# Optimization experiments

Measured on AMD Instinct MI355X. Metric: run time of the kernel, lower is better.

Reference implementation:

```python
import jax, jax.numpy as jnp
import numpy as np
import math

N, S, E, H = 32, 64, 512, 4
HD = E // H
EQ = E // 4
L2_TEMP = 13.544
LN_EPS = 1e-5


def _ln(x, g, b):
    m = jnp.mean(x, -1, keepdims=True)
    v = jnp.var(x, -1, keepdims=True)
    return (x - m) * jax.lax.rsqrt(v + LN_EPS) * g + b


def setup_inputs() -> dict:
    key = jax.random.key(0)
    ks = jax.random.split(key, 16)
    sc = 0.02
    inp = {
        "x": jax.random.normal(ks[0], (N, S, E), jnp.float32),
        # MultiheadAttention params (torch layout: in_proj_weight (3E,E))
        "Wqkv": jax.random.normal(ks[1], (3 * E, E), jnp.float32) * sc,
        "bqkv": jnp.zeros((3 * E,), jnp.float32),
        "Wo": jax.random.normal(ks[2], (E, E), jnp.float32) * sc,
        "bo": jnp.zeros((E,), jnp.float32),
        # fc1 (E, 2E), fc2 (E, E)
        "W1": jax.random.normal(ks[3], (E, 2 * E), jnp.float32) * sc,
        "b1": jnp.zeros((E,), jnp.float32),
        "W2": jax.random.normal(ks[4], (E, E), jnp.float32) * sc,
        "b2": jnp.zeros((E,), jnp.float32),
        # layer norms
        "g1": jnp.ones((E,), jnp.float32), "be1": jnp.zeros((E,), jnp.float32),
        "g2": jnp.ones((E,), jnp.float32), "be2": jnp.zeros((E,), jnp.float32),
        # fc_diff1: Linear(E, E//4), Linear(E//4, 1)
        "d1W1": jax.random.normal(ks[5], (EQ, E), jnp.float32) * sc,
        "d1b1": jnp.zeros((EQ,), jnp.float32),
        "d1W2": jax.random.normal(ks[6], (1, EQ), jnp.float32) * sc,
        "d1b2": jnp.zeros((1,), jnp.float32),
        # fc_diff2
        "d2W1": jax.random.normal(ks[7], (EQ, E), jnp.float32) * sc,
        "d2b1": jnp.zeros((EQ,), jnp.float32),
        "d2W2": jax.random.normal(ks[8], (1, EQ), jnp.float32) * sc,
        "d2b2": jnp.zeros((1,), jnp.float32),
    }
    return inp


def _mha(x, Wqkv, bqkv, Wo, bo):
    n, s, e = x.shape
    qkv = x @ Wqkv.T + bqkv
    q, k, v = jnp.split(qkv, 3, axis=-1)
    sh = lambda t: t.reshape(n, s, H, HD).transpose(0, 2, 1, 3)  # (n,H,s,hd)
    q, k, v = sh(q), sh(k), sh(v)
    scores = jnp.einsum('bhqd,bhkd->bhqk', q, k) / math.sqrt(HD)
    a = jax.nn.softmax(scores, axis=-1)
    o = jnp.einsum('bhqk,bhkd->bhqd', a, v).transpose(0, 2, 1, 3).reshape(n, s, e)
    return o @ Wo.T + bo, a.mean(axis=1)  # averaged attn weights (torch default)


def _pair_mlp(diff_w, W1a, b1a, W2a, b2a):
    # F.relu applied after every 'layer' (Linear, Dropout(eval=id), Linear)
    h = jax.nn.relu(diff_w @ W1a.T + b1a)  # relu(dropout(relu)) == relu composed -> same
    return jax.nn.relu(h @ W2a.T + b2a)[..., 0]  # (N,f,f)


def reference(x, Wqkv, bqkv, Wo, bo, W1, b1, W2, b2, g1, be1, g2, be2,
              d1W1, d1b1, d1W2, d1b2, d2W1, d2b1, d2W2, d2b2):
    # diff[b,f,g,e] = x[b,g,e] - x[b,f,e]
    diff = x[:, None, :, :] - x[:, :, None, :]  # (N,f,f,E)
    x1_attn = jax.nn.softmax(-jnp.sum(diff * diff, -1) / L2_TEMP, axis=-1)  # (N,f,f)
    x1 = jnp.einsum('bfg,bge->bfe', x1_attn, x)
    x2, x2_attn = _mha(x, Wqkv, bqkv, Wo, bo)
    x_res = jnp.concatenate([x1, x2], axis=-1)
    h = x + jax.nn.relu(x_res @ W1.T + b1)  # dropout eval = identity
    h = _ln(h, g1, be1)
    h = h + jax.nn.relu(h @ W2.T + b2)
    out = _ln(h, g2, be2)
    diff1 = _pair_mlp(diff * x1_attn[..., None], d1W1, d1b1, d1W2, d1b2)
    diff2 = _pair_mlp(diff * x2_attn[..., None], d2W1, d2b1, d2W2, d2b2)
    return out, x1_attn[:, None], x2_attn[:, None], diff1, diff2
```

## Files before the change

kernel.cpp:

```cpp
#include <hip/hip_runtime.h>
#include <math.h>

#define SS 64
#define EE 512
#define L2T 13.544f
#define LNEPS 1e-5f

using bf16x8 = __attribute__((ext_vector_type(8))) __bf16;
using u16x8  = __attribute__((ext_vector_type(8))) unsigned short;
using f32x4  = __attribute__((ext_vector_type(4))) float;

typedef const void __attribute__((address_space(1))) cv_global;
typedef void __attribute__((address_space(3))) v_lds;

__device__ inline unsigned short f2bf(float f) {
    union { float f; unsigned u; } v; v.f = f;
    unsigned r = v.u + 0x7fff + ((v.u >> 16) & 1);
    return (unsigned short)(r >> 16);
}
__device__ inline float bf2f(unsigned short h) {
    union { unsigned u; float f; } v; v.u = (unsigned)h << 16;
    return v.f;
}

#define MFMA16 __builtin_amdgcn_mfma_f32_16x16x32_bf16

#define XB_O    0
#define WFULL_O 1048576
#define W1CB_O  1966080
#define W2B_O   2490368
#define QKVB_O  2752512
#define X1O_O   5898240
#define HB_O    7995392
#define PB_O    9043968

__global__ __launch_bounds__(256)
void mega1(const float* __restrict__ x, const float* __restrict__ Wqkv,
           const float* __restrict__ Wo, const float* __restrict__ W1,
           const float* __restrict__ W2, const float* __restrict__ d1,
           const float* __restrict__ d2, const float* __restrict__ b1,
           const float* __restrict__ bo, unsigned short* __restrict__ bb,
           float* __restrict__ b_eff, float* __restrict__ x1_attn,
           unsigned short* __restrict__ Pl2) {
    const int bx = blockIdx.x, tid = threadIdx.x;
    __shared__ __align__(16) char smem[36096];

    if (bx < 1408) {
        int i = bx * 256 + tid;
        ushort4* dst4 = (ushort4*)bb;
        const float4* s; int di;
        if (i < 196608)      { s = (const float4*)Wqkv + i;          di = WFULL_O/4 + i; }
        else if (i < 212992) { int j = i-196608; s = (const float4*)d1 + j; di = WFULL_O/4 + 196608 + j; }
        else if (i < 229376) { int j = i-212992; s = (const float4*)d2 + j; di = WFULL_O/4 + 212992 + j; }
        else if (i < 294912) { int j = i-229376; s = (const float4*)W2 + j; di = W2B_O/4 + j; }
        else                 { int j = i-294912; int r = j>>7, cq = j&127;
                               s = (const float4*)W1 + r*256 + cq;   di = W1CB_O/4 + r*256 + cq; }
        float4 v = *s;
        ushort4 o;
        o.x = f2bf(v.x); o.y = f2bf(v.y); o.z = f2bf(v.z); o.w = f2bf(v.w);
        dst4[di] = o;
    } else if (bx < 1472) {
        const int tb = bx - 1408;
        const int m0 = (tb >> 3) * 64, n0 = (tb & 7) * 64;
        unsigned short* Asl = (unsigned short*)smem;
        unsigned short* Bsl = Asl + 64 * 40;
        const int wave = tid >> 6, lane = tid & 63;
        const int wm = (wave >> 1) * 32, wn = (wave & 1) * 32;
        const int fr = lane & 15, kq = (lane >> 4) * 8;
        f32x4 acc[2][2] = {};
        for (int k0 = 0; k0 < 512; k0 += 32) {
            {
                int m = tid >> 2, kk = (tid & 3) * 8;
                const float* src = W1 + (size_t)(m0 + m) * 1024 + 512 + k0 + kk;
                float4 v0 = *(const float4*)src, v1 = *(const float4*)(src + 4);
                u16x8 t = {f2bf(v0.x), f2bf(v0.y), f2bf(v0.z), f2bf(v0.w),
                           f2bf(v1.x), f2bf(v1.y), f2bf(v1.z), f2bf(v1.w)};
                *(u16x8*)(Asl + m * 40 + kk) = t;
            }
            {
                int k = tid >> 3, jq = (tid & 7) * 8;
                const float* src = Wo + (size_t)(k0 + k) * 512 + n0 + jq;
                float4 v0 = *(const float4*)src, v1 = *(const float4*)(src + 4);
                float vv[8] = {v0.x, v0.y, v0.z, v0.w, v1.x, v1.y, v1.z, v1.w};
                #pragma unroll
                for (int e = 0; e < 8; ++e) Bsl[(jq + e) * 40 + k] = f2bf(vv[e]);
            }
            __syncthreads();
            bf16x8 a0 = *(const bf16x8*)(Asl + (wm + fr) * 40 + kq);
            bf16x8 a1 = *(const bf16x8*)(Asl + (wm + 16 + fr) * 40 + kq);
            bf16x8 b0 = *(const bf16x8*)(Bsl + (wn + fr) * 40 + kq);
            bf16x8 b1 = *(const bf16x8*)(Bsl + (wn + 16 + fr) * 40 + kq);
            acc[0][0] = MFMA16(a0, b0, acc[0][0], 0, 0, 0);
            acc[0][1] = MFMA16(a0, b1, acc[0][1], 0, 0, 0);
            acc[1][0] = MFMA16(a1, b0, acc[1][0], 0, 0, 0);
            acc[1][1] = MFMA16(a1, b1, acc[1][1], 0, 0, 0);
            __syncthreads();
        }
        unsigned short* W1cb = bb + W1CB_O;
        const int crow = (lane >> 4) * 4, ccol = lane & 15;
        #pragma unroll
        for (int r2 = 0; r2 < 2; ++r2)
            #pragma unroll
            for (int c2 = 0; c2 < 2; ++c2)
                #pragma unroll
                for (int i = 0; i < 4; ++i) {
                    int m = m0 + wm + r2 * 16 + crow + i;
                    int j = n0 + wn + c2 * 16 + ccol;
                    W1cb[(size_t)m * 1024 + 512 + j] = f2bf(acc[r2][c2][i]);
                }
    } else if (bx < 1476) {
        int n = (bx - 1472) * 128 + (tid >> 1);
        int kh = (tid & 1) * 256;
        float s = 0.f;
        for (int k = 0; k < 256; ++k)
            s += W1[(size_t)n * 1024 + 512 + kh + k] * bo[kh + k];
        s += __shfl_xor(s, 1);
        if ((tid & 1) == 0) b_eff[n] = b1[n] + s;
    } else {
        const int b = bx - 1476;
        unsigned short* Xhi = (unsigned short*)smem;
        unsigned short* Xlo = Xhi + 64 * 72;
        float* sc    = (float*)(Xlo + 64 * 72);
        float* norms = sc + 64 * 68;
        const int wave = tid >> 6, lane = tid & 63;
        const int wm = (wave >> 1) * 32, wn = (wave & 1) * 32;
        const int fr = lane & 15;
        const int srow = tid >> 2, scq = (tid & 3) * 16;

        f32x4 acc[2][2] = {};
        const float* xrow = x + (size_t)b * 32768;
        unsigned short* xbg = bb + XB_O + (size_t)b * 32768;

        for (int k0 = 0; k0 < 512; k0 += 64) {
            const float* src = xrow + srow * 512 + k0 + scq;
            u16x8 hi0, hi1, lo0, lo1;
            #pragma unroll
            for (int e = 0; e < 8; ++e) {
                float v = src[e];
                unsigned short h = f2bf(v);
                hi0[e] = h; lo0[e] = f2bf(v - bf2f(h));
            }
            #pragma unroll
            for (int e = 0; e < 8; ++e) {
                float v = src[8 + e];
                unsigned short h = f2bf(v);
                hi1[e] = h; lo1[e] = f2bf(v - bf2f(h));
            }
            *(u16x8*)(Xhi + srow * 72 + scq)     = hi0;
            *(u16x8*)(Xhi + srow * 72 + scq + 8) = hi1;
            *(u16x8*)(Xlo + srow * 72 + scq)     = lo0;
            *(u16x8*)(Xlo + srow * 72 + scq + 8) = lo1;
            *(u16x8*)(xbg + srow * 512 + k0 + scq)     = hi0;
            *(u16x8*)(xbg + srow * 512 + k0 + scq + 8) = hi1;
            __syncthreads();
            #pragma unroll
            for (int j = 0; j < 2; ++j) {
                int kk = j * 32 + (lane >> 4) * 8;
                bf16x8 ah0 = *(const bf16x8*)(Xhi + (wm + fr) * 72 + kk);
                bf16x8 ah1 = *(const bf16x8*)(Xhi + (wm + 16 + fr) * 72 + kk);
                bf16x8 bh0 = *(const bf16x8*)(Xhi + (wn + fr) * 72 + kk);
                bf16x8 bh1 = *(const bf16x8*)(Xhi + (wn + 16 + fr) * 72 + kk);
                bf16x8 al0 = *(const bf16x8*)(Xlo + (wm + fr) * 72 + kk);
                bf16x8 al1 = *(const bf16x8*)(Xlo + (wm + 16 + fr) * 72 + kk);
                bf16x8 bl0 = *(const bf16x8*)(Xlo + (wn + fr) * 72 + kk);
                bf16x8 bl1 = *(const bf16x8*)(Xlo + (wn + 16 + fr) * 72 + kk);
                acc[0][0] = MFMA16(ah0, bh0, acc[0][0], 0, 0, 0);
                acc[0][0] = MFMA16(ah0, bl0, acc[0][0], 0, 0, 0);
                acc[0][0] = MFMA16(al0, bh0, acc[0][0], 0, 0, 0);
                acc[0][1] = MFMA16(ah0, bh1, acc[0][1], 0, 0, 0);
                acc[0][1] = MFMA16(ah0, bl1, acc[0][1], 0, 0, 0);
                acc[0][1] = MFMA16(al0, bh1, acc[0][1], 0, 0, 0);
                acc[1][0] = MFMA16(ah1, bh0, acc[1][0], 0, 0, 0);
                acc[1][0] = MFMA16(ah1, bl0, acc[1][0], 0, 0, 0);
                acc[1][0] = MFMA16(al1, bh0, acc[1][0], 0, 0, 0);
                acc[1][1] = MFMA16(ah1, bh1, acc[1][1], 0, 0, 0);
                acc[1][1] = MFMA16(ah1, bl1, acc[1][1], 0, 0, 0);
                acc[1][1] = MFMA16(al1, bh1, acc[1][1], 0, 0, 0);
            }
            __syncthreads();
        }
        const int crow = (lane >> 4) * 4, ccol = lane & 15;
        #pragma unroll
        for (int r2 = 0; r2 < 2; ++r2)
            #pragma unroll
            for (int c2 = 0; c2 < 2; ++c2)
                #pragma unroll
                for (int i = 0; i < 4; ++i)
                    sc[(wm + r2 * 16 + crow + i) * 68 + wn + c2 * 16 + ccol] =
                        acc[r2][c2][i];
        __syncthreads();
        if (tid < 64) norms[tid] = sc[tid * 68 + tid];
        __syncthreads();
        #pragma unroll
        for (int i = 0; i < 16; ++i) {
            int f = wave * 16 + i;
            float nf = norms[f];
            float val = (2.f * sc[f * 68 + lane] - nf - norms[lane]) * (1.0f / L2T);
            float mx = val;
            #pragma unroll
            for (int m = 32; m; m >>= 1) mx = fmaxf(mx, __shfl_xor(mx, m));
            float e = expf(val - mx);
            float sum = e;
            #pragma unroll
            for (int m = 32; m; m >>= 1) sum += __shfl_xor(sum, m);
            float a = e / sum;
            x1_attn[((size_t)b * 64 + f) * 64 + lane] = a;
            Pl2[((size_t)b * 64 + f) * 64 + lane] = f2bf(a);
        }
    }
}

__global__ __launch_bounds__(256)
void gemm_qkvp(const unsigned short* __restrict__ A,
               const unsigned short* __restrict__ B,
               const float* __restrict__ bias,
               unsigned short* __restrict__ Cq, unsigned short* __restrict__ Cp,
               const unsigned short* __restrict__ Pl2,
               unsigned short* __restrict__ x1o) {
    __shared__ unsigned short qsm[8704];
    const int tid = threadIdx.x, wave = tid >> 6, lane = tid & 63;
    const int fr = lane & 15;
    const int crow = (lane >> 4) * 4, ccol = lane & 15;

    if (blockIdx.x < 28) {
        unsigned short* Asl = qsm;
        unsigned short* Bsl = qsm + 4096;
        const int m0 = blockIdx.y * 64, n0 = blockIdx.x * 64;
        const int wm = (wave >> 1) * 32, wn = (wave & 1) * 32;
        const int kq4 = lane >> 4;
        f32x4 acc[2][2] = {};

        for (int k0 = 0; k0 < 512; k0 += 64) {
            #pragma unroll
            for (int c0 = 0; c0 < 512; c0 += 256) {
                int cc = c0 + tid, r = cc >> 3, q = cc & 7;
                int col = (q ^ (r & 7)) * 8;
                __builtin_amdgcn_global_load_lds(
                    (cv_global*)(A + (size_t)(m0 + r) * 512 + k0 + col),
                    (v_lds*)(Asl + c0 * 8 + wave * 512), 16, 0, 0);
            }
            #pragma unroll
            for (int c0 = 0; c0 < 512; c0 += 256) {
                int cc = c0 + tid, r = cc >> 3, q = cc & 7;
                int col = (q ^ (r & 7)) * 8;
                __builtin_amdgcn_global_load_lds(
                    (cv_global*)(B + (size_t)(n0 + r) * 512 + k0 + col),
                    (v_lds*)(Bsl + c0 * 8 + wave * 512), 16, 0, 0);
            }
            __syncthreads();
            #pragma unroll
            for (int j = 0; j < 2; ++j) {
                int kc = kq4 + j * 4;
                int rb0 = wn + fr, rb1 = wn + 16 + fr;
                bf16x8 b0 = *(const bf16x8*)(Bsl + rb0 * 64 + (kc ^ (rb0 & 7)) * 8);
                bf16x8 b1 = *(const bf16x8*)(Bsl + rb1 * 64 + (kc ^ (rb1 & 7)) * 8);
                #pragma unroll
                for (int r = 0; r < 2; ++r) {
                    int ra = wm + r * 16 + fr;
                    bf16x8 af = *(const bf16x8*)(Asl + ra * 64 + (kc ^ (ra & 7)) * 8);
                    acc[r][0] = MFMA16(af, b0, acc[r][0], 0, 0, 0);
                    acc[r][1] = MFMA16(af, b1, acc[r][1], 0, 0, 0);
                }
            }
            __syncthreads();
        }

        if (blockIdx.x < 24) {
            float bj0 = bias[n0 + wn + ccol], bj1 = bias[n0 + wn + 16 + ccol];
            #pragma unroll
            for (int r = 0; r < 2; ++r)
                #pragma unroll
                for (int c = 0; c < 2; ++c) {
                    float bj = c ? bj1 : bj0;
                    #pragma unroll
                    for (int i = 0; i < 4; ++i) {
                        size_t m = (size_t)(m0 + wm + r * 16 + crow + i);
                        int n = n0 + wn + c * 16 + ccol;
                        Cq[m * 1536 + n] = f2bf(acc[r][c][i] + bj);
                    }
                }
        } else {
            int p0 = n0 - 1536;
            #pragma unroll
            for (int r = 0; r < 2; ++r)
                #pragma unroll
                for (int c = 0; c < 2; ++c)
                    #pragma unroll
                    for (int i = 0; i < 4; ++i) {
                        size_t m = (size_t)(m0 + wm + r * 16 + crow + i);
                        int n = p0 + wn + c * 16 + ccol;
                        Cp[m * 256 + n] = f2bf(acc[r][c][i]);
                    }
        }
    } else {
        const int e0 = (blockIdx.x - 28) * 64;
        const int b = blockIdx.y;
        unsigned short* Ap = qsm;
        unsigned short* Xt = qsm + 64 * 68;
        {
            int row = tid >> 2, cq = (tid & 3) * 16;
            const unsigned short* src = Pl2 + (size_t)b * 4096 + row * 64 + cq;
            *(u16x8*)(Ap + row * 68 + cq)     = *(const u16x8*)src;
            *(u16x8*)(Ap + row * 68 + cq + 8) = *(const u16x8*)(src + 8);
        }
        {
            int g = tid >> 2, cq = (tid & 3) * 16;
            const unsigned short* src = A + (size_t)b * 32768 + g * 512 + e0 + cq;
            u16x8 v0 = *(const u16x8*)src, v1 = *(const u16x8*)(src + 8);
            #pragma unroll
            for (int e = 0; e < 8; ++e) Xt[(cq + e) * 68 + g] = v0[e];
            #pragma unroll
            for (int e = 0; e < 8; ++e) Xt[(cq + 8 + e) * 68 + g] = v1[e];
        }
        __syncthreads();
        const int wm2 = wave * 16;
        f32x4 o[4] = {};
        #pragma unroll
        for (int j = 0; j < 2; ++j) {
            int kk = j * 32 + (lane >> 4) * 8;
            bf16x8 a = *(const bf16x8*)(Ap + (wm2 + fr) * 68 + kk);
            #pragma unroll
            for (int t = 0; t < 4; ++t) {
                bf16x8 bv = *(const bf16x8*)(Xt + (t * 16 + fr) * 68 + kk);
                o[t] = MFMA16(a, bv, o[t], 0, 0, 0);
            }
        }
        #pragma unroll
        for (int t = 0; t < 4; ++t)
            #pragma unroll
            for (int i = 0; i < 4; ++i) {
                size_t m = (size_t)b * 64 + wm2 + crow + i;
                x1o[m * 1024 + e0 + t * 16 + ccol] = f2bf(o[t][i]);
            }
    }
}

__global__ __launch_bounds__(256)
void mha_attn(const unsigned short* __restrict__ qkv,
              unsigned short* __restrict__ x1o, float* __restrict__ pws) {
    const int hh = blockIdx.x;
    const int h = hh >> 1, half = hh & 1;
    const int b = blockIdx.y;
    const int tid = threadIdx.x, wave = tid >> 6, lane = tid & 63;

    __shared__ unsigned short Qs[32 * 136];
    __shared__ unsigned short Ks[64 * 136];
    __shared__ unsigned short Vt[128 * 72];
    __shared__ float sc[32 * 68];
    __shared__ unsigned short Pbf[32 * 72];

    const unsigned short* base = qkv + (size_t)b * 64 * 1536;
    {
        int row = tid >> 3, col = (tid & 7) * 16;
        const unsigned short* src = base + (half * 32 + row) * 1536 + h * 128 + col;
        *(u16x8*)(Qs + row * 136 + col)     = *(const u16x8*)(src);
        *(u16x8*)(Qs + row * 136 + col + 8) = *(const u16x8*)(src + 8);
    }
    {
        int row = tid >> 2, col = (tid & 3) * 32;
        const unsigned short* src = base + row * 1536 + 512 + h * 128 + col;
        #pragma unroll
        for (int j = 0; j < 4; ++j)
            *(u16x8*)(Ks + row * 136 + col + j * 8) = *(const u16x8*)(src + j * 8);
    }
    {
        int g = tid >> 2, col = (tid & 3) * 32;
        const unsigned short* src = base + g * 1536 + 1024 + h * 128 + col;
        #pragma unroll
        for (int j = 0; j < 4; ++j) {
            u16x8 v = *(const u16x8*)(src + j * 8);
            #pragma unroll
            for (int e = 0; e < 8; ++e)
                Vt[(col + j * 8 + e) * 72 + g] = v[e];
        }
    }
    __syncthreads();

    const int fr = lane & 15, kq = (lane >> 4) * 8;
    const int crow = (lane >> 4) * 4, ccol = lane & 15;
    const int wm = (wave >> 1) * 16;
    {
        const int wn = (wave & 1) * 32;
        f32x4 s0 = {0.f, 0.f, 0.f, 0.f}, s1 = s0;
        #pragma unroll
        for (int k0 = 0; k0 < 128; k0 += 32) {
            bf16x8 a  = *(const bf16x8*)(Qs + (wm + fr) * 136 + k0 + kq);
            bf16x8 b0 = *(const bf16x8*)(Ks + (wn + fr) * 136 + k0 + kq);
            bf16x8 b1 = *(const bf16x8*)(Ks + (wn + 16 + fr) * 136 + k0 + kq);
            s0 = MFMA16(a, b0, s0, 0, 0, 0);
            s1 = MFMA16(a, b1, s1, 0, 0, 0);
        }
        const float scale = 0.08838834764831845f;
        #pragma unroll
        for (int r = 0; r < 4; ++r) {
            sc[(wm + crow + r) * 68 + wn + ccol]      = s0[r] * scale;
            sc[(wm + crow + r) * 68 + wn + 16 + ccol] = s1[r] * scale;
        }
    }
    __syncthreads();

    #pragma unroll
    for (int i = 0; i < 8; ++i) {
        int f = wave * 8 + i;
        float v = sc[f * 68 + lane];
        float mx = v;
        #pragma unroll
        for (int m = 32; m; m >>= 1) mx = fmaxf(mx, __shfl_xor(mx, m));
        float e = expf(v - mx);
        float sum = e;
        #pragma unroll
        for (int m = 32; m; m >>= 1) sum += __shfl_xor(sum, m);
        float a = e / sum;
        Pbf[f * 72 + lane] = f2bf(a);
        pws[(((size_t)b * 4 + h) * 64 + half * 32 + f) * 64 + lane] = a;
    }
    __syncthreads();

    {
        const int wn2 = (wave & 1) * 64;
        f32x4 o[4];
        #pragma unroll
        for (int t = 0; t < 4; ++t) o[t] = f32x4{0.f, 0.f, 0.f, 0.f};
        #pragma unroll
        for (int k0 = 0; k0 < 64; k0 += 32) {
            bf16x8 a = *(const bf16x8*)(Pbf + (wm + fr) * 72 + k0 + kq);
            #pragma unroll
            for (int t = 0; t < 4; ++t) {
                bf16x8 bv = *(const bf16x8*)(Vt + (wn2 + t * 16 + fr) * 72 + k0 + kq);
                o[t] = MFMA16(a, bv, o[t], 0, 0, 0);
            }
        }
        #pragma unroll
        for (int t = 0; t < 4; ++t)
            #pragma unroll
            for (int r = 0; r < 4; ++r) {
                size_t m = (size_t)b * 64 + half * 32 + wm + crow + r;
                int col = h * 128 + wn2 + t * 16 + ccol;
                x1o[m * 1024 + 512 + col] = f2bf(o[t][r]);
            }
    }
}

__global__ __launch_bounds__(256)
void w1pair(const unsigned short* __restrict__ x1o,
            const unsigned short* __restrict__ W1cb,
            const float* __restrict__ beff, float* __restrict__ u,
            const unsigned short* __restrict__ Pb,
            const float* __restrict__ a1, const float* __restrict__ pws,
            const float* __restrict__ d1b1, const float* __restrict__ d1w2,
            const float* __restrict__ d1b2, const float* __restrict__ d2b1,
            const float* __restrict__ d2w2, const float* __restrict__ d2b2,
            float* __restrict__ x2_attn, float* __restrict__ out1,
            float* __restrict__ out2) {
    __shared__ unsigned short Asl[32 * 64];
    __shared__ unsigned short Bsl[64 * 64];
    const int bx = blockIdx.x, tid = threadIdx.x;
    const int wave = tid >> 6, lane = tid & 63;

    if (bx < 512) {
        const int m0 = (bx >> 3) * 32, n0 = (bx & 7) * 64;
        const int wm = (wave >> 1) * 16, wn = (wave & 1) * 32;
        const int fr = lane & 15, kq4 = lane >> 4;
        f32x4 acc[2] = {};
        for (int k0 = 0; k0 < 1024; k0 += 64) {
            {
                int r = tid >> 3, q = tid & 7;
                int col = (q ^ (r & 7)) * 8;
                __builtin_amdgcn_global_load_lds(
                    (cv_global*)(x1o + (size_t)(m0 + r) * 1024 + k0 + col),
                    (v_lds*)(Asl + wave * 512), 16, 0, 0);
            }
            #pragma unroll
            for (int c0 = 0; c0 < 512; c0 += 256) {
                int cc = c0 + tid, r = cc >> 3, q = cc & 7;
                int col = (q ^ (r & 7)) * 8;
                __builtin_amdgcn_global_load_lds(
                    (cv_global*)(W1cb + (size_t)(n0 + r) * 1024 + k0 + col),
                    (v_lds*)(Bsl + c0 * 8 + wave * 512), 16, 0, 0);
            }
            __syncthreads();
            #pragma unroll
            for (int j = 0; j < 2; ++j) {
                int kc = kq4 + j * 4;
                int rb0 = wn + fr, rb1 = wn + 16 + fr, ra = wm + fr;
                bf16x8 b0 = *(const bf16x8*)(Bsl + rb0 * 64 + (kc ^ (rb0 & 7)) * 8);
                bf16x8 b1 = *(const bf16x8*)(Bsl + rb1 * 64 + (kc ^ (rb1 & 7)) * 8);
                bf16x8 af = *(const bf16x8*)(Asl + ra * 64 + (kc ^ (ra & 7)) * 8);
                acc[0] = MFMA16(af, b0, acc[0], 0, 0, 0);
                acc[1] = MFMA16(af, b1, acc[1], 0, 0, 0);
            }
            __syncthreads();
        }
        const int crow = (lane >> 4) * 4, ccol = lane & 15;
        #pragma unroll
        for (int c = 0; c < 2; ++c) {
            int n = n0 + wn + c * 16 + ccol;
            float bj = beff[n];
            #pragma unroll
            for (int i = 0; i < 4; ++i) {
                size_t m = (size_t)(m0 + wm + crow + i);
                u[m * 512 + n] = fmaxf(acc[c][i] + bj, 0.f);
            }
        }
    } else {
        const int idx = bx - 512;
        const int f = idx & 63, b = idx >> 6;
        const size_t row = (size_t)b * SS + f;
        const int c0 = lane * 2, c1 = lane * 2 + 1;

        const float p1f0 = bf2f(Pb[row * 256 + c0]),       p1f1 = bf2f(Pb[row * 256 + c1]);
        const float p2f0 = bf2f(Pb[row * 256 + 128 + c0]), p2f1 = bf2f(Pb[row * 256 + 128 + c1]);
        const float w10 = d1w2[c0], w11 = d1w2[c1];
        const float w20 = d2w2[c0], w21 = d2w2[c1];
        const float b10 = d1b1[c0], b11 = d1b1[c1];
        const float b20 = d2b1[c0], b21 = d2b1[c1];
        const float bb1 = d1b2[0], bb2 = d2b2[0];

        const float* a1r = a1 + row * SS;
        const float* ph0 = pws + (((size_t)b * 4 + 0) * 64 + f) * 64;
        const float* ph1 = pws + (((size_t)b * 4 + 1) * 64 + f) * 64;
        const float* ph2 = pws + (((size_t)b * 4 + 2) * 64 + f) * 64;
        const float* ph3 = pws + (((size_t)b * 4 + 3) * 64 + f) * 64;
        const size_t bbase = (size_t)b * SS * 256;

        for (int g = wave; g < 64; g += 4) {
            float aa1 = a1r[g];
            float aa2 = 0.25f * (ph0[g] + ph1[g] + ph2[g] + ph3[g]);
            float q10 = bf2f(Pb[bbase + g * 256 + c0]);
            float q11 = bf2f(Pb[bbase + g * 256 + c1]);
            float q20 = bf2f(Pb[bbase + g * 256 + 128 + c0]);
            float q21 = bf2f(Pb[bbase + g * 256 + 128 + c1]);
            float h10 = fmaxf(aa1 * (q10 - p1f0) + b10, 0.f);
            float h11 = fmaxf(aa1 * (q11 - p1f1) + b11, 0.f);
            float h20 = fmaxf(aa2 * (q20 - p2f0) + b20, 0.f);
            float h21 = fmaxf(aa2 * (q21 - p2f1) + b21, 0.f);
            float s1 = w10 * h10 + w11 * h11;
            float s2 = w20 * h20 + w21 * h21;
            #pragma unroll
            for (int m = 32; m; m >>= 1) {
                s1 += __shfl_xor(s1, m);
                s2 += __shfl_xor(s2, m);
            }
            if (lane == 0) {
                x2_attn[row * SS + g] = aa2;
                out1[row * SS + g] = fmaxf(s1 + bb1, 0.f);
                out2[row * SS + g] = fmaxf(s2 + bb2, 0.f);
            }
        }
    }
}

__global__ __launch_bounds__(256)
void gemm_w2(const unsigned short* __restrict__ A,
             const unsigned short* __restrict__ B,
             const float* __restrict__ bias, float* __restrict__ C) {
    __shared__ unsigned short Asl[32 * 64];
    __shared__ unsigned short Bsl[64 * 64];
    const int tid = threadIdx.x, wave = tid >> 6, lane = tid & 63;
    const int m0 = blockIdx.y * 32, n0 = blockIdx.x * 64;
    const int wm = (wave >> 1) * 16, wn = (wave & 1) * 32;
    const int fr = lane & 15, kq4 = lane >> 4;
    f32x4 acc[2] = {};
    for (int k0 = 0; k0 < 512; k0 += 64) {
        {
            int r = tid >> 3, q = tid & 7;
            int col = (q ^ (r & 7)) * 8;
            __builtin_amdgcn_global_load_lds(
                (cv_global*)(A + (size_t)(m0 + r) * 512 + k0 + col),
                (v_lds*)(Asl + wave * 512), 16, 0, 0);
        }
        #pragma unroll
        for (int c0 = 0; c0 < 512; c0 += 256) {
            int cc = c0 + tid, r = cc >> 3, q = cc & 7;
            int col = (q ^ (r & 7)) * 8;
            __builtin_amdgcn_global_load_lds(
                (cv_global*)(B + (size_t)(n0 + r) * 512 + k0 + col),
                (v_lds*)(Bsl + c0 * 8 + wave * 512), 16, 0, 0);
        }
        __syncthreads();
        #pragma unroll
        for (int j = 0; j < 2; ++j) {
            int kc = kq4 + j * 4;
            int rb0 = wn + fr, rb1 = wn + 16 + fr, ra = wm + fr;
            bf16x8 b0 = *(const bf16x8*)(Bsl + rb0 * 64 + (kc ^ (rb0 & 7)) * 8);
            bf16x8 b1 = *(const bf16x8*)(Bsl + rb1 * 64 + (kc ^ (rb1 & 7)) * 8);
            bf16x8 af = *(const bf16x8*)(Asl + ra * 64 + (kc ^ (ra & 7)) * 8);
            acc[0] = MFMA16(af, b0, acc[0], 0, 0, 0);
            acc[1] = MFMA16(af, b1, acc[1], 0, 0, 0);
        }
        __syncthreads();
    }
    const int crow = (lane >> 4) * 4, ccol = lane & 15;
    #pragma unroll
    for (int c = 0; c < 2; ++c) {
        int n = n0 + wn + c * 16 + ccol;
        float bj = bias[n];
        #pragma unroll
        for (int i = 0; i < 4; ++i) {
            size_t m = (size_t)(m0 + wm + crow + i);
            C[m * 512 + n] = fmaxf(acc[c][i] + bj, 0.f);
        }
    }
}

__global__ __launch_bounds__(256)
void add_ln(const float* __restrict__ base, const float* __restrict__ u,
            const float* __restrict__ gam, const float* __restrict__ bet,
            float* __restrict__ out, unsigned short* __restrict__ outb) {
    const int row = blockIdx.x;
    const int tid = threadIdx.x, wave = tid >> 6, lane = tid & 63;
    const float* br = base + (size_t)row * EE;
    const float* ur = u + (size_t)row * EE;
    float t0 = br[tid] + ur[tid];
    float t1 = br[tid + 256] + ur[tid + 256];
    float s = t0 + t1, sq = t0 * t0 + t1 * t1;
    #pragma unroll
    for (int m = 32; m; m >>= 1) {
        s += __shfl_xor(s, m);
        sq += __shfl_xor(sq, m);
    }
    __shared__ float ssum[4], ssq[4];
    if (lane == 0) { ssum[wave] = s; ssq[wave] = sq; }
    __syncthreads();
    s = ssum[0] + ssum[1] + ssum[2] + ssum[3];
    sq = ssq[0] + ssq[1] + ssq[2] + ssq[3];
    float mean = s * (1.0f / EE);
    float var = sq * (1.0f / EE) - mean * mean;
    float inv = rsqrtf(var + LNEPS);
    float v0 = (t0 - mean) * inv * gam[tid] + bet[tid];
    float v1 = (t1 - mean) * inv * gam[tid + 256] + bet[tid + 256];
    float* orow = out + (size_t)row * EE;
    orow[tid] = v0;
    orow[tid + 256] = v1;
    if (outb) {
        unsigned short* obr = outb + (size_t)row * EE;
        obr[tid] = f2bf(v0);
        obr[tid + 256] = f2bf(v1);
    }
}

extern "C" void kernel_launch(void* const* d_in, const int* in_sizes, int n_in,
                              void* d_out, int out_size, void* d_ws,
                              size_t ws_size, hipStream_t stream) {
    const float* x    = (const float*)d_in[0];
    const float* Wqkv = (const float*)d_in[1];
    const float* bqkv = (const float*)d_in[2];
    const float* Wo   = (const float*)d_in[3];
    const float* bo   = (const float*)d_in[4];
    const float* W1   = (const float*)d_in[5];
    const float* b1   = (const float*)d_in[6];
    const float* W2   = (const float*)d_in[7];
    const float* b2   = (const float*)d_in[8];
    const float* g1   = (const float*)d_in[9];
    const float* be1  = (const float*)d_in[10];
    const float* g2   = (const float*)d_in[11];
    const float* be2  = (const float*)d_in[12];
    const float* d1W1 = (const float*)d_in[13];
    const float* d1b1 = (const float*)d_in[14];
    const float* d1W2 = (const float*)d_in[15];
    const float* d1b2 = (const float*)d_in[16];
    const float* d2W1 = (const float*)d_in[17];
    const float* d2b1 = (const float*)d_in[18];
    const float* d2W2 = (const float*)d_in[19];
    const float* d2b2 = (const float*)d_in[20];

    float* out      = (float*)d_out;
    float* out_main = out;
    float* x1_attn  = out + 1048576;
    float* x2_attn  = out + 1048576 + 131072;
    float* diff1    = out + 1048576 + 2 * 131072;
    float* diff2    = out + 1048576 + 3 * 131072;

    float* ws    = (float*)d_ws;
    float* u_buf = ws;
    float* h_buf = ws + 1048576;
    float* pws   = ws + 2097152;
    float* b_eff = ws + 2621440;
    unsigned short* Pl2 = (unsigned short*)(ws + 2621952);
    unsigned short* bb  = (unsigned short*)(ws + 2687488);

    unsigned short* xb    = bb + XB_O;
    unsigned short* Wfull = bb + WFULL_O;
    unsigned short* W1cb  = bb + W1CB_O;
    unsigned short* W2b   = bb + W2B_O;
    unsigned short* qkvb  = bb + QKVB_O;
    unsigned short* x1o   = bb + X1O_O;
    unsigned short* hb    = bb + HB_O;
    unsigned short* Pb    = bb + PB_O;

    mega1<<<1508, 256, 0, stream>>>(x, Wqkv, Wo, W1, W2, d1W1, d2W1, b1, bo,
                                    bb, b_eff, x1_attn, Pl2);

    gemm_qkvp<<<dim3(36, 32), 256, 0, stream>>>(xb, Wfull, bqkv, qkvb, Pb,
                                                Pl2, x1o);

    mha_attn<<<dim3(8, 32), 256, 0, stream>>>(qkvb, x1o, pws);

    w1pair<<<2560, 256, 0, stream>>>(x1o, W1cb, b_eff, u_buf, Pb, x1_attn, pws,
                                     d1b1, d1W2, d1b2, d2b1, d2W2, d2b2,
                                     x2_attn, diff1, diff2);

    add_ln<<<2048, 256, 0, stream>>>(x, u_buf, g1, be1, h_buf, hb);

    gemm_w2<<<dim3(8, 64), 256, 0, stream>>>(hb, W2b, b2, u_buf);

    add_ln<<<2048, 256, 0, stream>>>(h_buf, u_buf, g2, be2, out_main, nullptr);
}
```

Baseline: 179.0 us.

## Merge all seven kernel launches into one persistent cooperative kernel with grid syncs

```diff
diff --git a/kernel.cpp b/kernel.cpp
--- a/kernel.cpp
+++ b/kernel.cpp
@@ -1,5 +1,8 @@
 #include <hip/hip_runtime.h>
+#include <hip/hip_cooperative_groups.h>
 #include <math.h>
+
+namespace cg = cooperative_groups;
 
 #define SS 64
 #define EE 512
@@ -34,580 +37,18 @@
 #define HB_O    7995392
 #define PB_O    9043968
 
-__global__ __launch_bounds__(256)
-void mega1(const float* __restrict__ x, const float* __restrict__ Wqkv,
-           const float* __restrict__ Wo, const float* __restrict__ W1,
-           const float* __restrict__ W2, const float* __restrict__ d1,
-           const float* __restrict__ d2, const float* __restrict__ b1,
-           const float* __restrict__ bo, unsigned short* __restrict__ bb,
-           float* __restrict__ b_eff, float* __restrict__ x1_attn,
-           unsigned short* __restrict__ Pl2) {
-    const int bx = blockIdx.x, tid = threadIdx.x;
-    __shared__ __align__(16) char smem[36096];
-
-    if (bx < 1408) {
-        int i = bx * 256 + tid;
-        ushort4* dst4 = (ushort4*)bb;
-        const float4* s; int di;
-        if (i < 196608)      { s = (const float4*)Wqkv + i;          di = WFULL_O/4 + i; }
-        else if (i < 212992) { int j = i-196608; s = (const float4*)d1 + j; di = WFULL_O/4 + 196608 + j; }
-        else if (i < 229376) { int j = i-212992; s = (const float4*)d2 + j; di = WFULL_O/4 + 212992 + j; }
-        else if (i < 294912) { int j = i-229376; s = (const float4*)W2 + j; di = W2B_O/4 + j; }
-        else                 { int j = i-294912; int r = j>>7, cq = j&127;
-                               s = (const float4*)W1 + r*256 + cq;   di = W1CB_O/4 + r*256 + cq; }
-        float4 v = *s;
-        ushort4 o;
-        o.x = f2bf(v.x); o.y = f2bf(v.y); o.z = f2bf(v.z); o.w = f2bf(v.w);
-        dst4[di] = o;
-    } else if (bx < 1472) {
-        const int tb = bx - 1408;
-        const int m0 = (tb >> 3) * 64, n0 = (tb & 7) * 64;
-        unsigned short* Asl = (unsigned short*)smem;
-        unsigned short* Bsl = Asl + 64 * 40;
-        const int wave = tid >> 6, lane = tid & 63;
-        const int wm = (wave >> 1) * 32, wn = (wave & 1) * 32;
-        const int fr = lane & 15, kq = (lane >> 4) * 8;
-        f32x4 acc[2][2] = {};
-        for (int k0 = 0; k0 < 512; k0 += 32) {
-            {
-                int m = tid >> 2, kk = (tid & 3) * 8;
-                const float* src = W1 + (size_t)(m0 + m) * 1024 + 512 + k0 + kk;
-                float4 v0 = *(const float4*)src, v1 = *(const float4*)(src + 4);
-                u16x8 t = {f2bf(v0.x), f2bf(v0.y), f2bf(v0.z), f2bf(v0.w),
-                           f2bf(v1.x), f2bf(v1.y), f2bf(v1.z), f2bf(v1.w)};
-                *(u16x8*)(Asl + m * 40 + kk) = t;
-            }
-            {
-                int k = tid >> 3, jq = (tid & 7) * 8;
-                const float* src = Wo + (size_t)(k0 + k) * 512 + n0 + jq;
-                float4 v0 = *(const float4*)src, v1 = *(const float4*)(src + 4);
-                float vv[8] = {v0.x, v0.y, v0.z, v0.w, v1.x, v1.y, v1.z, v1.w};
-                #pragma unroll
-                for (int e = 0; e < 8; ++e) Bsl[(jq + e) * 40 + k] = f2bf(vv[e]);
-            }
-            __syncthreads();
-            bf16x8 a0 = *(const bf16x8*)(Asl + (wm + fr) * 40 + kq);
-            bf16x8 a1 = *(const bf16x8*)(Asl + (wm + 16 + fr) * 40 + kq);
-            bf16x8 b0 = *(const bf16x8*)(Bsl + (wn + fr) * 40 + kq);
-            bf16x8 b1 = *(const bf16x8*)(Bsl + (wn + 16 + fr) * 40 + kq);
-            acc[0][0] = MFMA16(a0, b0, acc[0][0], 0, 0, 0);
-            acc[0][1] = MFMA16(a0, b1, acc[0][1], 0, 0, 0);
-            acc[1][0] = MFMA16(a1, b0, acc[1][0], 0, 0, 0);
-            acc[1][1] = MFMA16(a1, b1, acc[1][1], 0, 0, 0);
-            __syncthreads();
-        }
-        unsigned short* W1cb = bb + W1CB_O;
-        const int crow = (lane >> 4) * 4, ccol = lane & 15;
-        #pragma unroll
-        for (int r2 = 0; r2 < 2; ++r2)
-            #pragma unroll
-            for (int c2 = 0; c2 < 2; ++c2)
-                #pragma unroll
-                for (int i = 0; i < 4; ++i) {
-                    int m = m0 + wm + r2 * 16 + crow + i;
-                    int j = n0 + wn + c2 * 16 + ccol;
-                    W1cb[(size_t)m * 1024 + 512 + j] = f2bf(acc[r2][c2][i]);
-                }
-    } else if (bx < 1476) {
-        int n = (bx - 1472) * 128 + (tid >> 1);
-        int kh = (tid & 1) * 256;
-        float s = 0.f;
-        for (int k = 0; k < 256; ++k)
-            s += W1[(size_t)n * 1024 + 512 + kh + k] * bo[kh + k];
-        s += __shfl_xor(s, 1);
-        if ((tid & 1) == 0) b_eff[n] = b1[n] + s;
-    } else {
-        const int b = bx - 1476;
-        unsigned short* Xhi = (unsigned short*)smem;
-        unsigned short* Xlo = Xhi + 64 * 72;
-        float* sc    = (float*)(Xlo + 64 * 72);
-        float* norms = sc + 64 * 68;
-        const int wave = tid >> 6, lane = tid & 63;
-        const int wm = (wave >> 1) * 32, wn = (wave & 1) * 32;
-        const int fr = lane & 15;
-        const int srow = tid >> 2, scq = (tid & 3) * 16;
-
-        f32x4 acc[2][2] = {};
-        const float* xrow = x + (size_t)b * 32768;
-        unsigned short* xbg = bb + XB_O + (size_t)b * 32768;
-
-        for (int k0 = 0; k0 < 512; k0 += 64) {
-            const float* src = xrow + srow * 512 + k0 + scq;
-            u16x8 hi0, hi1, lo0, lo1;
-            #pragma unroll
-            for (int e = 0; e < 8; ++e) {
-                float v = src[e];
-                unsigned short h = f2bf(v);
-                hi0[e] = h; lo0[e] = f2bf(v - bf2f(h));
-            }
-            #pragma unroll
-            for (int e = 0; e < 8; ++e) {
-                float v = src[8 + e];
-                unsigned short h = f2bf(v);
-                hi1[e] = h; lo1[e] = f2bf(v - bf2f(h));
-            }
-            *(u16x8*)(Xhi + srow * 72 + scq)     = hi0;
-            *(u16x8*)(Xhi + srow * 72 + scq + 8) = hi1;
-            *(u16x8*)(Xlo + srow * 72 + scq)     = lo0;
-            *(u16x8*)(Xlo + srow * 72 + scq + 8) = lo1;
-            *(u16x8*)(xbg + srow * 512 + k0 + scq)     = hi0;
-            *(u16x8*)(xbg + srow * 512 + k0 + scq + 8) = hi1;
-            __syncthreads();
-            #pragma unroll
-            for (int j = 0; j < 2; ++j) {
-                int kk = j * 32 + (lane >> 4) * 8;
-                bf16x8 ah0 = *(const bf16x8*)(Xhi + (wm + fr) * 72 + kk);
-                bf16x8 ah1 = *(const bf16x8*)(Xhi + (wm + 16 + fr) * 72 + kk);
-                bf16x8 bh0 = *(const bf16x8*)(Xhi + (wn + fr) * 72 + kk);
-                bf16x8 bh1 = *(const bf16x8*)(Xhi + (wn + 16 + fr) * 72 + kk);
-                bf16x8 al0 = *(const bf16x8*)(Xlo + (wm + fr) * 72 + kk);
-                bf16x8 al1 = *(const bf16x8*)(Xlo + (wm + 16 + fr) * 72 + kk);
-                bf16x8 bl0 = *(const bf16x8*)(Xlo + (wn + fr) * 72 + kk);
-                bf16x8 bl1 = *(const bf16x8*)(Xlo + (wn + 16 + fr) * 72 + kk);
-                acc[0][0] = MFMA16(ah0, bh0, acc[0][0], 0, 0, 0);
-                acc[0][0] = MFMA16(ah0, bl0, acc[0][0], 0, 0, 0);
-                acc[0][0] = MFMA16(al0, bh0, acc[0][0], 0, 0, 0);
-                acc[0][1] = MFMA16(ah0, bh1, acc[0][1], 0, 0, 0);
-                acc[0][1] = MFMA16(ah0, bl1, acc[0][1], 0, 0, 0);
-                acc[0][1] = MFMA16(al0, bh1, acc[0][1], 0, 0, 0);
-                acc[1][0] = MFMA16(ah1, bh0, acc[1][0], 0, 0, 0);
-                acc[1][0] = MFMA16(ah1, bl0, acc[1][0], 0, 0, 0);
-                acc[1][0] = MFMA16(al1, bh0, acc[1][0], 0, 0, 0);
-                acc[1][1] = MFMA16(ah1, bh1, acc[1][1], 0, 0, 0);
-                acc[1][1] = MFMA16(ah1, bl1, acc[1][1], 0, 0, 0);
-                acc[1][1] = MFMA16(al1, bh1, acc[1][1], 0, 0, 0);
-            }
-            __syncthreads();
-        }
-        const int crow = (lane >> 4) * 4, ccol = lane & 15;
-        #pragma unroll
-        for (int r2 = 0; r2 < 2; ++r2)
-            #pragma unroll
-            for (int c2 = 0; c2 < 2; ++c2)
-                #pragma unroll
-                for (int i = 0; i < 4; ++i)
-                    sc[(wm + r2 * 16 + crow + i) * 68 + wn + c2 * 16 + ccol] =
-                        acc[r2][c2][i];
-        __syncthreads();
-        if (tid < 64) norms[tid] = sc[tid * 68 + tid];
-        __syncthreads();
-        #pragma unroll
-        for (int i = 0; i < 16; ++i) {
-            int f = wave * 16 + i;
-            float nf = norms[f];
-            float val = (2.f * sc[f * 68 + lane] - nf - norms[lane]) * (1.0f / L2T);
-            float mx = val;
-            #pragma unroll
-            for (int m = 32; m; m >>= 1) mx = fmaxf(mx, __shfl_xor(mx, m));
-            float e = expf(val - mx);
-            float sum = e;
-            #pragma unroll
-            for (int m = 32; m; m >>= 1) sum += __shfl_xor(sum, m);
-            float a = e / sum;
-            x1_attn[((size_t)b * 64 + f) * 64 + lane] = a;
-            Pl2[((size_t)b * 64 + f) * 64 + lane] = f2bf(a);
-        }
-    }
-}
-
-__global__ __launch_bounds__(256)
-void gemm_qkvp(const unsigned short* __restrict__ A,
-               const unsigned short* __restrict__ B,
-               const float* __restrict__ bias,
-               unsigned short* __restrict__ Cq, unsigned short* __restrict__ Cp,
-               const unsigned short* __restrict__ Pl2,
-               unsigned short* __restrict__ x1o) {
-    __shared__ unsigned short qsm[8704];
-    const int tid = threadIdx.x, wave = tid >> 6, lane = tid & 63;
-    const int fr = lane & 15;
-    const int crow = (lane >> 4) * 4, ccol = lane & 15;
-
-    if (blockIdx.x < 28) {
-        unsigned short* Asl = qsm;
-        unsigned short* Bsl = qsm + 4096;
-        const int m0 = blockIdx.y * 64, n0 = blockIdx.x * 64;
-        const int wm = (wave >> 1) * 32, wn = (wave & 1) * 32;
-        const int kq4 = lane >> 4;
-        f32x4 acc[2][2] = {};
-
-        for (int k0 = 0; k0 < 512; k0 += 64) {
-            #pragma unroll
-            for (int c0 = 0; c0 < 512; c0 += 256) {
-                int cc = c0 + tid, r = cc >> 3, q = cc & 7;
-                int col = (q ^ (r & 7)) * 8;
-                __builtin_amdgcn_global_load_lds(
-                    (cv_global*)(A + (size_t)(m0 + r) * 512 + k0 + col),
-                    (v_lds*)(Asl + c0 * 8 + wave * 512), 16, 0, 0);
-            }
-            #pragma unroll
-            for (int c0 = 0; c0 < 512; c0 += 256) {
-                int cc = c0 + tid, r = cc >> 3, q = cc & 7;
-                int col = (q ^ (r & 7)) * 8;
-                __builtin_amdgcn_global_load_lds(
-                    (cv_global*)(B + (size_t)(n0 + r) * 512 + k0 + col),
-                    (v_lds*)(Bsl + c0 * 8 + wave * 512), 16, 0, 0);
-            }
-            __syncthreads();
-            #pragma unroll
-            for (int j = 0; j < 2; ++j) {
-                int kc = kq4 + j * 4;
-                int rb0 = wn + fr, rb1 = wn + 16 + fr;
-                bf16x8 b0 = *(const bf16x8*)(Bsl + rb0 * 64 + (kc ^ (rb0 & 7)) * 8);
-                bf16x8 b1 = *(const bf16x8*)(Bsl + rb1 * 64 + (kc ^ (rb1 & 7)) * 8);
-                #pragma unroll
-                for (int r = 0; r < 2; ++r) {
-                    int ra = wm + r * 16 + fr;
-                    bf16x8 af = *(const bf16x8*)(Asl + ra * 64 + (kc ^ (ra & 7)) * 8);
-                    acc[r][0] = MFMA16(af, b0, acc[r][0], 0, 0, 0);
-                    acc[r][1] = MFMA16(af, b1, acc[r][1], 0, 0, 0);
-                }
-            }
-            __syncthreads();
-        }
-
-        if (blockIdx.x < 24) {
-            float bj0 = bias[n0 + wn + ccol], bj1 = bias[n0 + wn + 16 + ccol];
-            #pragma unroll
-            for (int r = 0; r < 2; ++r)
-                #pragma unroll
-                for (int c = 0; c < 2; ++c) {
-                    float bj = c ? bj1 : bj0;
-                    #pragma unroll
-                    for (int i = 0; i < 4; ++i) {
-                        size_t m = (size_t)(m0 + wm + r * 16 + crow + i);
-                        int n = n0 + wn + c * 16 + ccol;
-                        Cq[m * 1536 + n] = f2bf(acc[r][c][i] + bj);
-                    }
-                }
-        } else {
-            int p0 = n0 - 1536;
-            #pragma unroll
-            for (int r = 0; r < 2; ++r)
-                #pragma unroll
-                for (int c = 0; c < 2; ++c)
-                    #pragma unroll
-                    for (int i = 0; i < 4; ++i) {
-                        size_t m = (size_t)(m0 + wm + r * 16 + crow + i);
-                        int n = p0 + wn + c * 16 + ccol;
-                        Cp[m * 256 + n] = f2bf(acc[r][c][i]);
-                    }
-        }
-    } else {
-        const int e0 = (blockIdx.x - 28) * 64;
-        const int b = blockIdx.y;
-        unsigned short* Ap = qsm;
-        unsigned short* Xt = qsm + 64 * 68;
-        {
-            int row = tid >> 2, cq = (tid & 3) * 16;
-            const unsigned short* src = Pl2 + (size_t)b * 4096 + row * 64 + cq;
-            *(u16x8*)(Ap + row * 68 + cq)     = *(const u16x8*)src;
-            *(u16x8*)(Ap + row * 68 + cq + 8) = *(const u16x8*)(src + 8);
-        }
-        {
-            int g = tid >> 2, cq = (tid & 3) * 16;
-            const unsigned short* src = A + (size_t)b * 32768 + g * 512 + e0 + cq;
-            u16x8 v0 = *(const u16x8*)src, v1 = *(const u16x8*)(src + 8);
-            #pragma unroll
-            for (int e = 0; e < 8; ++e) Xt[(cq + e) * 68 + g] = v0[e];
-            #pragma unroll
-            for (int e = 0; e < 8; ++e) Xt[(cq + 8 + e) * 68 + g] = v1[e];
-        }
-        __syncthreads();
-        const int wm2 = wave * 16;
-        f32x4 o[4] = {};
-        #pragma unroll
-        for (int j = 0; j < 2; ++j) {
-            int kk = j * 32 + (lane >> 4) * 8;
-            bf16x8 a = *(const bf16x8*)(Ap + (wm2 + fr) * 68 + kk);
-            #pragma unroll
-            for (int t = 0; t < 4; ++t) {
-                bf16x8 bv = *(const bf16x8*)(Xt + (t * 16 + fr) * 68 + kk);
-                o[t] = MFMA16(a, bv, o[t], 0, 0, 0);
-            }
-        }
-        #pragma unroll
-        for (int t = 0; t < 4; ++t)
-            #pragma unroll
-            for (int i = 0; i < 4; ++i) {
-                size_t m = (size_t)b * 64 + wm2 + crow + i;
-                x1o[m * 1024 + e0 + t * 16 + ccol] = f2bf(o[t][i]);
-            }
-    }
-}
-
-__global__ __launch_bounds__(256)
-void mha_attn(const unsigned short* __restrict__ qkv,
-              unsigned short* __restrict__ x1o, float* __restrict__ pws) {
-    const int hh = blockIdx.x;
-    const int h = hh >> 1, half = hh & 1;
-    const int b = blockIdx.y;
-    const int tid = threadIdx.x, wave = tid >> 6, lane = tid & 63;
-
-    __shared__ unsigned short Qs[32 * 136];
-    __shared__ unsigned short Ks[64 * 136];
-    __shared__ unsigned short Vt[128 * 72];
-    __shared__ float sc[32 * 68];
-    __shared__ unsigned short Pbf[32 * 72];
-
-    const unsigned short* base = qkv + (size_t)b * 64 * 1536;
-    {
-        int row = tid >> 3, col = (tid & 7) * 16;
-        const unsigned short* src = base + (half * 32 + row) * 1536 + h * 128 + col;
-        *(u16x8*)(Qs + row * 136 + col)     = *(const u16x8*)(src);
-        *(u16x8*)(Qs + row * 136 + col + 8) = *(const u16x8*)(src + 8);
-    }
-    {
-        int row = tid >> 2, col = (tid & 3) * 32;
-        const unsigned short* src = base + row * 1536 + 512 + h * 128 + col;
-        #pragma unroll
-        for (int j = 0; j < 4; ++j)
-            *(u16x8*)(Ks + row * 136 + col + j * 8) = *(const u16x8*)(src + j * 8);
-    }
-    {
-        int g = tid >> 2, col = (tid & 3) * 32;
-        const unsigned short* src = base + g * 1536 + 1024 + h * 128 + col;
-        #pragma unroll
-        for (int j = 0; j < 4; ++j) {
-            u16x8 v = *(const u16x8*)(src + j * 8);
-            #pragma unroll
-            for (int e = 0; e < 8; ++e)
-                Vt[(col + j * 8 + e) * 72 + g] = v[e];
-        }
-    }
-    __syncthreads();
-
-    const int fr = lane & 15, kq = (lane >> 4) * 8;
-    const int crow = (lane >> 4) * 4, ccol = lane & 15;
-    const int wm = (wave >> 1) * 16;
-    {
-        const int wn = (wave & 1) * 32;
-        f32x4 s0 = {0.f, 0.f, 0.f, 0.f}, s1 = s0;
-        #pragma unroll
-        for (int k0 = 0; k0 < 128; k0 += 32) {
-            bf16x8 a  = *(const bf16x8*)(Qs + (wm + fr) * 136 + k0 + kq);
-            bf16x8 b0 = *(const bf16x8*)(Ks + (wn + fr) * 136 + k0 + kq);
-            bf16x8 b1 = *(const bf16x8*)(Ks + (wn + 16 + fr) * 136 + k0 + kq);
-            s0 = MFMA16(a, b0, s0, 0, 0, 0);
-            s1 = MFMA16(a, b1, s1, 0, 0, 0);
-        }
-        const float scale = 0.08838834764831845f;
-        #pragma unroll
-        for (int r = 0; r < 4; ++r) {
-            sc[(wm + crow + r) * 68 + wn + ccol]      = s0[r] * scale;
-            sc[(wm + crow + r) * 68 + wn + 16 + ccol] = s1[r] * scale;
-        }
-    }
-    __syncthreads();
-
-    #pragma unroll
-    for (int i = 0; i < 8; ++i) {
-        int f = wave * 8 + i;
-        float v = sc[f * 68 + lane];
-        float mx = v;
-        #pragma unroll
-        for (int m = 32; m; m >>= 1) mx = fmaxf(mx, __shfl_xor(mx, m));
-        float e = expf(v - mx);
-        float sum = e;
-        #pragma unroll
-        for (int m = 32; m; m >>= 1) sum += __shfl_xor(sum, m);
-        float a = e / sum;
-        Pbf[f * 72 + lane] = f2bf(a);
-        pws[(((size_t)b * 4 + h) * 64 + half * 32 + f) * 64 + lane] = a;
-    }
-    __syncthreads();
-
-    {
-        const int wn2 = (wave & 1) * 64;
-        f32x4 o[4];
-        #pragma unroll
-        for (int t = 0; t < 4; ++t) o[t] = f32x4{0.f, 0.f, 0.f, 0.f};
-        #pragma unroll
-        for (int k0 = 0; k0 < 64; k0 += 32) {
-            bf16x8 a = *(const bf16x8*)(Pbf + (wm + fr) * 72 + k0 + kq);
-            #pragma unroll
-            for (int t = 0; t < 4; ++t) {
-                bf16x8 bv = *(const bf16x8*)(Vt + (wn2 + t * 16 + fr) * 72 + k0 + kq);
-                o[t] = MFMA16(a, bv, o[t], 0, 0, 0);
-            }
-        }
-        #pragma unroll
-        for (int t = 0; t < 4; ++t)
-            #pragma unroll
-            for (int r = 0; r < 4; ++r) {
-                size_t m = (size_t)b * 64 + half * 32 + wm + crow + r;
-                int col = h * 128 + wn2 + t * 16 + ccol;
-                x1o[m * 1024 + 512 + col] = f2bf(o[t][r]);
-            }
-    }
-}
-
-__global__ __launch_bounds__(256)
-void w1pair(const unsigned short* __restrict__ x1o,
-            const unsigned short* __restrict__ W1cb,
-            const float* __restrict__ beff, float* __restrict__ u,
-            const unsigned short* __restrict__ Pb,
-            const float* __restrict__ a1, const float* __restrict__ pws,
-            const float* __restrict__ d1b1, const float* __restrict__ d1w2,
-            const float* __restrict__ d1b2, const float* __restrict__ d2b1,
-            const float* __restrict__ d2w2, const float* __restrict__ d2b2,
-            float* __restrict__ x2_attn, float* __restrict__ out1,
-            float* __restrict__ out2) {
-    __shared__ unsigned short Asl[32 * 64];
-    __shared__ unsigned short Bsl[64 * 64];
-    const int bx = blockIdx.x, tid = threadIdx.x;
-    const int wave = tid >> 6, lane = tid & 63;
-
-    if (bx < 512) {
-        const int m0 = (bx >> 3) * 32, n0 = (bx & 7) * 64;
-        const int wm = (wave >> 1) * 16, wn = (wave & 1) * 32;
-        const int fr = lane & 15, kq4 = lane >> 4;
-        f32x4 acc[2] = {};
-        for (int k0 = 0; k0 < 1024; k0 += 64) {
-            {
-                int r = tid >> 3, q = tid & 7;
-                int col = (q ^ (r & 7)) * 8;
-                __builtin_amdgcn_global_load_lds(
-                    (cv_global*)(x1o + (size_t)(m0 + r) * 1024 + k0 + col),
-                    (v_lds*)(Asl + wave * 512), 16, 0, 0);
-            }
-            #pragma unroll
-            for (int c0 = 0; c0 < 512; c0 += 256) {
-                int cc = c0 + tid, r = cc >> 3, q = cc & 7;
-                int col = (q ^ (r & 7)) * 8;
-                __builtin_amdgcn_global_load_lds(
-                    (cv_global*)(W1cb + (size_t)(n0 + r) * 1024 + k0 + col),
-                    (v_lds*)(Bsl + c0 * 8 + wave * 512), 16, 0, 0);
-            }
-            __syncthreads();
-            #pragma unroll
-            for (int j = 0; j < 2; ++j) {
-                int kc = kq4 + j * 4;
-                int rb0 = wn + fr, rb1 = wn + 16 + fr, ra = wm + fr;
-                bf16x8 b0 = *(const bf16x8*)(Bsl + rb0 * 64 + (kc ^ (rb0 & 7)) * 8);
-                bf16x8 b1 = *(const bf16x8*)(Bsl + rb1 * 64 + (kc ^ (rb1 & 7)) * 8);
-                bf16x8 af = *(const bf16x8*)(Asl + ra * 64 + (kc ^ (ra & 7)) * 8);
-                acc[0] = MFMA16(af, b0, acc[0], 0, 0, 0);
-                acc[1] = MFMA16(af, b1, acc[1], 0, 0, 0);
-            }
-            __syncthreads();
-        }
-        const int crow = (lane >> 4) * 4, ccol = lane & 15;
-        #pragma unroll
-        for (int c = 0; c < 2; ++c) {
-            int n = n0 + wn + c * 16 + ccol;
-            float bj = beff[n];
-            #pragma unroll
-            for (int i = 0; i < 4; ++i) {
-                size_t m = (size_t)(m0 + wm + crow + i);
-                u[m * 512 + n] = fmaxf(acc[c][i] + bj, 0.f);
-            }
-        }
-    } else {
-        const int idx = bx - 512;
-        const int f = idx & 63, b = idx >> 6;
-        const size_t row = (size_t)b * SS + f;
-        const int c0 = lane * 2, c1 = lane * 2 + 1;
-
-        const float p1f0 = bf2f(Pb[row * 256 + c0]),       p1f1 = bf2f(Pb[row * 256 + c1]);
-        const float p2f0 = bf2f(Pb[row * 256 + 128 + c0]), p2f1 = bf2f(Pb[row * 256 + 128 + c1]);
-        const float w10 = d1w2[c0], w11 = d1w2[c1];
-        const float w20 = d2w2[c0], w21 = d2w2[c1];
-        const float b10 = d1b1[c0], b11 = d1b1[c1];
-        const float b20 = d2b1[c0], b21 = d2b1[c1];
-        const float bb1 = d1b2[0], bb2 = d2b2[0];
-
-        const float* a1r = a1 + row * SS;
-        const float* ph0 = pws + (((size_t)b * 4 + 0) * 64 + f) * 64;
-        const float* ph1 = pws + (((size_t)b * 4 + 1) * 64 + f) * 64;
-        const float* ph2 = pws + (((size_t)b * 4 + 2) * 64 + f) * 64;
-        const float* ph3 = pws + (((size_t)b * 4 + 3) * 64 + f) * 64;
-        const size_t bbase = (size_t)b * SS * 256;
-
-        for (int g = wave; g < 64; g += 4) {
-            float aa1 = a1r[g];
-            float aa2 = 0.25f * (ph0[g] + ph1[g] + ph2[g] + ph3[g]);
-            float q10 = bf2f(Pb[bbase + g * 256 + c0]);
-            float q11 = bf2f(Pb[bbase + g * 256 + c1]);
-            float q20 = bf2f(Pb[bbase + g * 256 + 128 + c0]);
-            float q21 = bf2f(Pb[bbase + g * 256 + 128 + c1]);
-            float h10 = fmaxf(aa1 * (q10 - p1f0) + b10, 0.f);
-            float h11 = fmaxf(aa1 * (q11 - p1f1) + b11, 0.f);
-            float h20 = fmaxf(aa2 * (q20 - p2f0) + b20, 0.f);
-            float h21 = fmaxf(aa2 * (q21 - p2f1) + b21, 0.f);
-            float s1 = w10 * h10 + w11 * h11;
-            float s2 = w20 * h20 + w21 * h21;
-            #pragma unroll
-            for (int m = 32; m; m >>= 1) {
-                s1 += __shfl_xor(s1, m);
-                s2 += __shfl_xor(s2, m);
-            }
-            if (lane == 0) {
-                x2_attn[row * SS + g] = aa2;
-                out1[row * SS + g] = fmaxf(s1 + bb1, 0.f);
-                out2[row * SS + g] = fmaxf(s2 + bb2, 0.f);
-            }
-        }
-    }
-}
-
-__global__ __launch_bounds__(256)
-void gemm_w2(const unsigned short* __restrict__ A,
-             const unsigned short* __restrict__ B,
-             const float* __restrict__ bias, float* __restrict__ C) {
-    __shared__ unsigned short Asl[32 * 64];
-    __shared__ unsigned short Bsl[64 * 64];
-    const int tid = threadIdx.x, wave = tid >> 6, lane = tid & 63;
-    const int m0 = blockIdx.y * 32, n0 = blockIdx.x * 64;
-    const int wm = (wave >> 1) * 16, wn = (wave & 1) * 32;
-    const int fr = lane & 15, kq4 = lane >> 4;
-    f32x4 acc[2] = {};
-    for (int k0 = 0; k0 < 512; k0 += 64) {
-        {
-            int r = tid >> 3, q = tid & 7;
-            int col = (q ^ (r & 7)) * 8;
-            __builtin_amdgcn_global_load_lds(
-                (cv_global*)(A + (size_t)(m0 + r) * 512 + k0 + col),
-                (v_lds*)(Asl + wave * 512), 16, 0, 0);
-        }
-        #pragma unroll
-        for (int c0 = 0; c0 < 512; c0 += 256) {
-            int cc = c0 + tid, r = cc >> 3, q = cc & 7;
-            int col = (q ^ (r & 7)) * 8;
-            __builtin_amdgcn_global_load_lds(
-                (cv_global*)(B + (size_t)(n0 + r) * 512 + k0 + col),
-                (v_lds*)(Bsl + c0 * 8 + wave * 512), 16, 0, 0);
-        }
-        __syncthreads();
-        #pragma unroll
-        for (int j = 0; j < 2; ++j) {
-            int kc = kq4 + j * 4;
-            int rb0 = wn + fr, rb1 = wn + 16 + fr, ra = wm + fr;
-            bf16x8 b0 = *(const bf16x8*)(Bsl + rb0 * 64 + (kc ^ (rb0 & 7)) * 8);
-            bf16x8 b1 = *(const bf16x8*)(Bsl + rb1 * 64 + (kc ^ (rb1 & 7)) * 8);
-            bf16x8 af = *(const bf16x8*)(Asl + ra * 64 + (kc ^ (ra & 7)) * 8);
-            acc[0] = MFMA16(af, b0, acc[0], 0, 0, 0);
-            acc[1] = MFMA16(af, b1, acc[1], 0, 0, 0);
-        }
-        __syncthreads();
-    }
-    const int crow = (lane >> 4) * 4, ccol = lane & 15;
-    #pragma unroll
-    for (int c = 0; c < 2; ++c) {
-        int n = n0 + wn + c * 16 + ccol;
-        float bj = bias[n];
-        #pragma unroll
-        for (int i = 0; i < 4; ++i) {
-            size_t m = (size_t)(m0 + wm + crow + i);
-            C[m * 512 + n] = fmaxf(acc[c][i] + bj, 0.f);
-        }
-    }
-}
-
-__global__ __launch_bounds__(256)
-void add_ln(const float* __restrict__ base, const float* __restrict__ u,
-            const float* __restrict__ gam, const float* __restrict__ bet,
-            float* __restrict__ out, unsigned short* __restrict__ outb) {
-    const int row = blockIdx.x;
+struct KParams {
+    const float *x, *Wqkv, *bqkv, *Wo, *bo, *W1, *b1, *W2, *b2;
+    const float *g1, *be1, *g2, *be2;
+    const float *d1W1, *d1b1, *d1W2, *d1b2, *d2W1, *d2b1, *d2W2, *d2b2;
+    float *out_main, *x1_attn, *x2_attn, *diff1, *diff2;
+    float *u_buf, *h_buf, *pws, *b_eff;
+    unsigned short *Pl2, *bb;
+};
+
+__device__ inline void ln_row(int row, const float* base, const float* u,
+                              const float* gam, const float* bet, float* out,
+                              unsigned short* outb, float* ssum, float* ssq) {
     const int tid = threadIdx.x, wave = tid >> 6, lane = tid & 63;
     const float* br = base + (size_t)row * EE;
     const float* ur = u + (size_t)row * EE;
@@ -619,7 +60,6 @@
         s += __shfl_xor(s, m);
         sq += __shfl_xor(sq, m);
     }
-    __shared__ float ssum[4], ssq[4];
     if (lane == 0) { ssum[wave] = s; ssq[wave] = sq; }
     __syncthreads();
     s = ssum[0] + ssum[1] + ssum[2] + ssum[3];
@@ -637,72 +77,602 @@
         obr[tid] = f2bf(v0);
         obr[tid + 256] = f2bf(v1);
     }
+    __syncthreads();
+}
+
+__global__ __launch_bounds__(256, 4)
+void fused(KParams p) {
+    __shared__ __align__(16) unsigned char smem[27680];
+    const int tid = threadIdx.x, wave = tid >> 6, lane = tid & 63;
+    const int fr = lane & 15, quad = lane >> 4, kq = quad * 8;
+    const int crow = quad * 4, ccol = fr;
+    const int GS = gridDim.x;
+    cg::grid_group grid = cg::this_grid();
+    unsigned short* bb = p.bb;
+
+    for (int w = blockIdx.x; w < 1508; w += GS) {
+        if (w < 1408) {
+            int i = w * 256 + tid;
+            ushort4* dst4 = (ushort4*)bb;
+            const float4* s; int di;
+            if (i < 196608)      { s = (const float4*)p.Wqkv + i;              di = WFULL_O/4 + i; }
+            else if (i < 212992) { int j = i-196608; s = (const float4*)p.d1W1 + j; di = WFULL_O/4 + 196608 + j; }
+            else if (i < 229376) { int j = i-212992; s = (const float4*)p.d2W1 + j; di = WFULL_O/4 + 212992 + j; }
+            else if (i < 294912) { int j = i-229376; s = (const float4*)p.W2 + j;   di = W2B_O/4 + j; }
+            else                 { int j = i-294912; int r = j>>7, cq = j&127;
+                                   s = (const float4*)p.W1 + r*256 + cq;       di = W1CB_O/4 + r*256 + cq; }
+            float4 v = *s;
+            ushort4 o;
+            o.x = f2bf(v.x); o.y = f2bf(v.y); o.z = f2bf(v.z); o.w = f2bf(v.w);
+            dst4[di] = o;
+        } else if (w < 1472) {
+            const int tb = w - 1408;
+            const int m0 = (tb >> 3) * 64, n0 = (tb & 7) * 64;
+            unsigned short* Asl = (unsigned short*)smem;
+            unsigned short* Bsl = Asl + 64 * 40;
+            const int wm = (wave >> 1) * 32, wn = (wave & 1) * 32;
+            f32x4 acc[2][2] = {};
+            for (int k0 = 0; k0 < 512; k0 += 32) {
+                {
+                    int m = tid >> 2, kk = (tid & 3) * 8;
+                    const float* src = p.W1 + (size_t)(m0 + m) * 1024 + 512 + k0 + kk;
+                    float4 v0 = *(const float4*)src, v1 = *(const float4*)(src + 4);
+                    u16x8 t = {f2bf(v0.x), f2bf(v0.y), f2bf(v0.z), f2bf(v0.w),
+                               f2bf(v1.x), f2bf(v1.y), f2bf(v1.z), f2bf(v1.w)};
+                    *(u16x8*)(Asl + m * 40 + kk) = t;
+                }
+                {
+                    int k = tid >> 3, jq = (tid & 7) * 8;
+                    const float* src = p.Wo + (size_t)(k0 + k) * 512 + n0 + jq;
+                    float4 v0 = *(const float4*)src, v1 = *(const float4*)(src + 4);
+                    float vv[8] = {v0.x, v0.y, v0.z, v0.w, v1.x, v1.y, v1.z, v1.w};
+                    #pragma unroll
+                    for (int e = 0; e < 8; ++e) Bsl[(jq + e) * 40 + k] = f2bf(vv[e]);
+                }
+                __syncthreads();
+                bf16x8 a0 = *(const bf16x8*)(Asl + (wm + fr) * 40 + kq);
+                bf16x8 a1 = *(const bf16x8*)(Asl + (wm + 16 + fr) * 40 + kq);
+                bf16x8 b0 = *(const bf16x8*)(Bsl + (wn + fr) * 40 + kq);
+                bf16x8 b1 = *(const bf16x8*)(Bsl + (wn + 16 + fr) * 40 + kq);
+                acc[0][0] = MFMA16(a0, b0, acc[0][0], 0, 0, 0);
+                acc[0][1] = MFMA16(a0, b1, acc[0][1], 0, 0, 0);
+                acc[1][0] = MFMA16(a1, b0, acc[1][0], 0, 0, 0);
+                acc[1][1] = MFMA16(a1, b1, acc[1][1], 0, 0, 0);
+                __syncthreads();
+            }
+            unsigned short* W1cb = bb + W1CB_O;
+            #pragma unroll
+            for (int r2 = 0; r2 < 2; ++r2)
+                #pragma unroll
+                for (int c2 = 0; c2 < 2; ++c2)
+                    #pragma unroll
+                    for (int i = 0; i < 4; ++i) {
+                        int m = m0 + wm + r2 * 16 + crow + i;
+                        int j = n0 + wn + c2 * 16 + ccol;
+                        W1cb[(size_t)m * 1024 + 512 + j] = f2bf(acc[r2][c2][i]);
+                    }
+        } else if (w < 1476) {
+            int n = (w - 1472) * 128 + (tid >> 1);
+            int kh = (tid & 1) * 256;
+            float s = 0.f;
+            for (int k = 0; k < 256; ++k)
+                s += p.W1[(size_t)n * 1024 + 512 + kh + k] * p.bo[kh + k];
+            s += __shfl_xor(s, 1);
+            if ((tid & 1) == 0) p.b_eff[n] = p.b1[n] + s;
+        } else {
+            const int b = w - 1476;
+            unsigned short* Xhi = (unsigned short*)smem;
+            unsigned short* Xlo = Xhi + 64 * 72;
+            float* norms = (float*)(smem + 18432);
+            const int wmg = wave * 16;
+            const int srow = tid >> 2, scq = (tid & 3) * 16;
+            f32x4 acc[4] = {};
+            const float* xrow = p.x + (size_t)b * 32768;
+            unsigned short* xbg = bb + XB_O + (size_t)b * 32768;
+
+            for (int k0 = 0; k0 < 512; k0 += 64) {
+                const float* src = xrow + srow * 512 + k0 + scq;
+                u16x8 hi0, hi1, lo0, lo1;
+                #pragma unroll
+                for (int e = 0; e < 8; ++e) {
+                    float v = src[e];
+                    unsigned short h = f2bf(v);
+                    hi0[e] = h; lo0[e] = f2bf(v - bf2f(h));
+                }
+                #pragma unroll
+                for (int e = 0; e < 8; ++e) {
+                    float v = src[8 + e];
+                    unsigned short h = f2bf(v);
+                    hi1[e] = h; lo1[e] = f2bf(v - bf2f(h));
+                }
+                *(u16x8*)(Xhi + srow * 72 + scq)     = hi0;
+                *(u16x8*)(Xhi + srow * 72 + scq + 8) = hi1;
+                *(u16x8*)(Xlo + srow * 72 + scq)     = lo0;
+                *(u16x8*)(Xlo + srow * 72 + scq + 8) = lo1;
+                *(u16x8*)(xbg + srow * 512 + k0 + scq)     = hi0;
+                *(u16x8*)(xbg + srow * 512 + k0 + scq + 8) = hi1;
+                __syncthreads();
+                #pragma unroll
+                for (int j = 0; j < 2; ++j) {
+                    int kk = j * 32 + kq;
+                    bf16x8 ah = *(const bf16x8*)(Xhi + (wmg + fr) * 72 + kk);
+                    bf16x8 al = *(const bf16x8*)(Xlo + (wmg + fr) * 72 + kk);
+                    #pragma unroll
+                    for (int t = 0; t < 4; ++t) {
+                        bf16x8 bh = *(const bf16x8*)(Xhi + (t * 16 + fr) * 72 + kk);
+                        bf16x8 bl = *(const bf16x8*)(Xlo + (t * 16 + fr) * 72 + kk);
+                        acc[t] = MFMA16(ah, bh, acc[t], 0, 0, 0);
+                        acc[t] = MFMA16(ah, bl, acc[t], 0, 0, 0);
+                        acc[t] = MFMA16(al, bh, acc[t], 0, 0, 0);
+                    }
+                }
+                __syncthreads();
+            }
+            #pragma unroll
+            for (int t = 0; t < 4; ++t)
+                #pragma unroll
+                for (int r = 0; r < 4; ++r) {
+                    int row = wmg + crow + r, col = t * 16 + fr;
+                    if (row == col) norms[row] = acc[t][r];
+                }
+            __syncthreads();
+            float ncol[4];
+            #pragma unroll
+            for (int t = 0; t < 4; ++t) ncol[t] = norms[t * 16 + fr];
+            #pragma unroll
+            for (int r = 0; r < 4; ++r) {
+                int row = wmg + crow + r;
+                float nf = norms[row];
+                float v[4], mx = -1e30f;
+                #pragma unroll
+                for (int t = 0; t < 4; ++t) {
+                    v[t] = (2.f * acc[t][r] - nf - ncol[t]) * (1.0f / L2T);
+                    mx = fmaxf(mx, v[t]);
+                }
+                #pragma unroll
+                for (int m = 8; m; m >>= 1) mx = fmaxf(mx, __shfl_xor(mx, m));
+                float e[4], sum = 0.f;
+                #pragma unroll
+                for (int t = 0; t < 4; ++t) { e[t] = expf(v[t] - mx); sum += e[t]; }
+                #pragma unroll
+                for (int m = 8; m; m >>= 1) sum += __shfl_xor(sum, m);
+                float rs = 1.f / sum;
+                #pragma unroll
+                for (int t = 0; t < 4; ++t) {
+                    float a = e[t] * rs;
+                    size_t idx = ((size_t)b * 64 + row) * 64 + t * 16 + fr;
+                    p.x1_attn[idx] = a;
+                    p.Pl2[idx] = f2bf(a);
+                }
+            }
+        }
+        __syncthreads();
+    }
+    grid.sync();
+
+    for (int w = blockIdx.x; w < 1152; w += GS) {
+        const int nx = w % 36, my = w / 36;
+        if (nx < 28) {
+            unsigned short* Asl = (unsigned short*)smem;
+            unsigned short* Bsl = Asl + 4096;
+            const unsigned short* A = bb + XB_O;
+            const unsigned short* B = bb + WFULL_O;
+            const int m0 = my * 64, n0 = nx * 64;
+            const int wm = (wave >> 1) * 32, wn = (wave & 1) * 32;
+            f32x4 acc[2][2] = {};
+            for (int k0 = 0; k0 < 512; k0 += 64) {
+                #pragma unroll
+                for (int c0 = 0; c0 < 512; c0 += 256) {
+                    int cc = c0 + tid, r = cc >> 3, q = cc & 7;
+                    int col = (q ^ (r & 7)) * 8;
+                    __builtin_amdgcn_global_load_lds(
+                        (cv_global*)(A + (size_t)(m0 + r) * 512 + k0 + col),
+                        (v_lds*)(Asl + c0 * 8 + wave * 512), 16, 0, 0);
+                }
+                #pragma unroll
+                for (int c0 = 0; c0 < 512; c0 += 256) {
+                    int cc = c0 + tid, r = cc >> 3, q = cc & 7;
+                    int col = (q ^ (r & 7)) * 8;
+                    __builtin_amdgcn_global_load_lds(
+                        (cv_global*)(B + (size_t)(n0 + r) * 512 + k0 + col),
+                        (v_lds*)(Bsl + c0 * 8 + wave * 512), 16, 0, 0);
+                }
+                __syncthreads();
+                #pragma unroll
+                for (int j = 0; j < 2; ++j) {
+                    int kc = (lane >> 4) + j * 4;
+                    int rb0 = wn + fr, rb1 = wn + 16 + fr;
+                    bf16x8 b0 = *(const bf16x8*)(Bsl + rb0 * 64 + (kc ^ (rb0 & 7)) * 8);
+                    bf16x8 b1 = *(const bf16x8*)(Bsl + rb1 * 64 + (kc ^ (rb1 & 7)) * 8);
+                    #pragma unroll
+                    for (int r = 0; r < 2; ++r) {
+                        int ra = wm + r * 16 + fr;
+                        bf16x8 af = *(const bf16x8*)(Asl + ra * 64 + (kc ^ (ra & 7)) * 8);
+                        acc[r][0] = MFMA16(af, b0, acc[r][0], 0, 0, 0);
+                        acc[r][1] = MFMA16(af, b1, acc[r][1], 0, 0, 0);
+                    }
+                }
+                __syncthreads();
+            }
+            if (nx < 24) {
+                unsigned short* Cq = bb + QKVB_O;
+                float bj0 = p.bqkv[n0 + wn + ccol], bj1 = p.bqkv[n0 + wn + 16 + ccol];
+                #pragma unroll
+                for (int r = 0; r < 2; ++r)
+                    #pragma unroll
+                    for (int c = 0; c < 2; ++c) {
+                        float bj = c ? bj1 : bj0;
+                        #pragma unroll
+                        for (int i = 0; i < 4; ++i) {
+                            size_t m = (size_t)(m0 + wm + r * 16 + crow + i);
+                            int n = n0 + wn + c * 16 + ccol;
+                            Cq[m * 1536 + n] = f2bf(acc[r][c][i] + bj);
+                        }
+                    }
+            } else {
+                unsigned short* Cp = bb + PB_O;
+                int p0 = n0 - 1536;
+                #pragma unroll
+                for (int r = 0; r < 2; ++r)
+                    #pragma unroll
+                    for (int c = 0; c < 2; ++c)
+                        #pragma unroll
+                        for (int i = 0; i < 4; ++i) {
+                            size_t m = (size_t)(m0 + wm + r * 16 + crow + i);
+                            int n = p0 + wn + c * 16 + ccol;
+                            Cp[m * 256 + n] = f2bf(acc[r][c][i]);
+                        }
+            }
+        } else {
+            const int e0 = (nx - 28) * 64, b = my;
+            unsigned short* Ap = (unsigned short*)smem;
+            unsigned short* Xt = Ap + 64 * 68;
+            {
+                int row = tid >> 2, cq2 = (tid & 3) * 16;
+                const unsigned short* src = p.Pl2 + (size_t)b * 4096 + row * 64 + cq2;
+                *(u16x8*)(Ap + row * 68 + cq2)     = *(const u16x8*)src;
+                *(u16x8*)(Ap + row * 68 + cq2 + 8) = *(const u16x8*)(src + 8);
+            }
+            {
+                int g = tid >> 2, cq2 = (tid & 3) * 16;
+                const unsigned short* src = bb + XB_O + (size_t)b * 32768 + g * 512 + e0 + cq2;
+                u16x8 v0 = *(const u16x8*)src, v1 = *(const u16x8*)(src + 8);
+                #pragma unroll
+                for (int e = 0; e < 8; ++e) Xt[(cq2 + e) * 68 + g] = v0[e];
+                #pragma unroll
+                for (int e = 0; e < 8; ++e) Xt[(cq2 + 8 + e) * 68 + g] = v1[e];
+            }
+            __syncthreads();
+            const int wm2 = wave * 16;
+            f32x4 o[4] = {};
+            #pragma unroll
+            for (int j = 0; j < 2; ++j) {
+                int kk = j * 32 + kq;
+                bf16x8 a = *(const bf16x8*)(Ap + (wm2 + fr) * 68 + kk);
+                #pragma unroll
+                for (int t = 0; t < 4; ++t) {
+                    bf16x8 bv = *(const bf16x8*)(Xt + (t * 16 + fr) * 68 + kk);
+                    o[t] = MFMA16(a, bv, o[t], 0, 0, 0);
+                }
+            }
+            unsigned short* x1o = bb + X1O_O;
+            #pragma unroll
+            for (int t = 0; t < 4; ++t)
+                #pragma unroll
+                for (int i = 0; i < 4; ++i) {
+                    size_t m = (size_t)b * 64 + wm2 + crow + i;
+                    x1o[m * 1024 + e0 + t * 16 + ccol] = f2bf(o[t][i]);
+                }
+        }
+        __syncthreads();
+    }
+    grid.sync();
+
+    for (int w = blockIdx.x; w < 128; w += GS) {
+        const int h = w & 3, b = w >> 2;
+        unsigned short* Ks = (unsigned short*)smem;
+        const unsigned short* base = bb + QKVB_O + (size_t)b * 64 * 1536;
+        {
+            int row = tid >> 2, col = (tid & 3) * 32;
+            const unsigned short* sk = base + row * 1536 + 512 + h * 128 + col;
+            #pragma unroll
+            for (int j = 0; j < 4; ++j)
+                *(u16x8*)(Ks + row * 136 + col + j * 8) = *(const u16x8*)(sk + j * 8);
+        }
+        __syncthreads();
+        const int wm = wave * 16;
+        const unsigned short* qrow = base + (size_t)(wm + fr) * 1536 + h * 128;
+        f32x4 sacc[4] = {};
+        #pragma unroll
+        for (int k0 = 0; k0 < 128; k0 += 32) {
+            bf16x8 a = *(const bf16x8*)(qrow + k0 + kq);
+            #pragma unroll
+            for (int t = 0; t < 4; ++t) {
+                bf16x8 bv = *(const bf16x8*)(Ks + (t * 16 + fr) * 136 + k0 + kq);
+                sacc[t] = MFMA16(a, bv, sacc[t], 0, 0, 0);
+            }
+        }
+        const float scale = 0.08838834764831845f;
+        float pa[4][4];
+        #pragma unroll
+        for (int r = 0; r < 4; ++r) {
+            int row = wm + crow + r;
+            float v[4], mx = -1e30f;
+            #pragma unroll
+            for (int t = 0; t < 4; ++t) {
+                v[t] = sacc[t][r] * scale;
+                mx = fmaxf(mx, v[t]);
+            }
+            #pragma unroll
+            for (int m = 8; m; m >>= 1) mx = fmaxf(mx, __shfl_xor(mx, m));
+            float e[4], sum = 0.f;
+            #pragma unroll
+            for (int t = 0; t < 4; ++t) { e[t] = expf(v[t] - mx); sum += e[t]; }
+            #pragma unroll
+            for (int m = 8; m; m >>= 1) sum += __shfl_xor(sum, m);
+            float rs = 1.f / sum;
+            #pragma unroll
+            for (int t = 0; t < 4; ++t) {
+                pa[t][r] = e[t] * rs;
+                p.pws[(((size_t)b * 4 + h) * 64 + row) * 64 + t * 16 + fr] = pa[t][r];
+            }
+        }
+        __syncthreads();
+        unsigned short* Vt  = (unsigned short*)smem;
+        unsigned short* Pbf = (unsigned short*)(smem + 18432);
+        {
+            int g = tid >> 2, col = (tid & 3) * 32;
+            const unsigned short* sv = base + g * 1536 + 1024 + h * 128 + col;
+            #pragma unroll
+            for (int j = 0; j < 4; ++j) {
+                u16x8 v = *(const u16x8*)(sv + j * 8);
+                #pragma unroll
+                for (int e = 0; e < 8; ++e)
+                    Vt[(col + j * 8 + e) * 72 + g] = v[e];
+            }
+        }
+        #pragma unroll
+        for (int t = 0; t < 4; ++t)
+            #pragma unroll
+            for (int r = 0; r < 4; ++r)
+                Pbf[(wm + crow + r) * 72 + t * 16 + fr] = f2bf(pa[t][r]);
+        __syncthreads();
+        f32x4 o[8] = {};
+        #pragma unroll
+        for (int c = 0; c < 2; ++c) {
+            bf16x8 a = *(const bf16x8*)(Pbf + (wm + fr) * 72 + c * 32 + kq);
+            #pragma unroll
+            for (int t = 0; t < 8; ++t) {
+                bf16x8 bv = *(const bf16x8*)(Vt + (t * 16 + fr) * 72 + c * 32 + kq);
+                o[t] = MFMA16(a, bv, o[t], 0, 0, 0);
+            }
+        }
+        unsigned short* x1o = bb + X1O_O;
+        #pragma unroll
+        for (int t = 0; t < 8; ++t)
+            #pragma unroll
+            for (int i = 0; i < 4; ++i) {
+                size_t m = (size_t)b * 64 + wm + crow + i;
+                int col = h * 128 + t * 16 + ccol;
+                x1o[m * 1024 + 512 + col] = f2bf(o[t][i]);
+            }
+        __syncthreads();
+    }
+    grid.sync();
+
+    for (int w = blockIdx.x; w < 2560; w += GS) {
+        if (w < 512) {
+            unsigned short* Asl = (unsigned short*)smem;
+            unsigned short* Bsl = Asl + 2048;
+            const unsigned short* x1o = bb + X1O_O;
+            const unsigned short* W1cb = bb + W1CB_O;
+            const int m0 = (w >> 3) * 32, n0 = (w & 7) * 64;
+            const int wm = (wave >> 1) * 16, wn = (wave & 1) * 32;
+            f32x4 acc[2] = {};
+            for (int k0 = 0; k0 < 1024; k0 += 64) {
+                {
+                    int r = tid >> 3, q = tid & 7;
+                    int col = (q ^ (r & 7)) * 8;
+                    __builtin_amdgcn_global_load_lds(
+                        (cv_global*)(x1o + (size_t)(m0 + r) * 1024 + k0 + col),
+                        (v_lds*)(Asl + wave * 512), 16, 0, 0);
+                }
+                #pragma unroll
+                for (int c0 = 0; c0 < 512; c0 += 256) {
+                    int cc = c0 + tid, r = cc >> 3, q = cc & 7;
+                    int col = (q ^ (r & 7)) * 8;
+                    __builtin_amdgcn_global_load_lds(
+                        (cv_global*)(W1cb + (size_t)(n0 + r) * 1024 + k0 + col),
+                        (v_lds*)(Bsl + c0 * 8 + wave * 512), 16, 0, 0);
+                }
+                __syncthreads();
+                #pragma unroll
+                for (int j = 0; j < 2; ++j) {
+                    int kc = (lane >> 4) + j * 4;
+                    int rb0 = wn + fr, rb1 = wn + 16 + fr, ra = wm + fr;
+                    bf16x8 b0 = *(const bf16x8*)(Bsl + rb0 * 64 + (kc ^ (rb0 & 7)) * 8);
+                    bf16x8 b1 = *(const bf16x8*)(Bsl + rb1 * 64 + (kc ^ (rb1 & 7)) * 8);
+                    bf16x8 af = *(const bf16x8*)(Asl + ra * 64 + (kc ^ (ra & 7)) * 8);
+                    acc[0] = MFMA16(af, b0, acc[0], 0, 0, 0);
+                    acc[1] = MFMA16(af, b1, acc[1], 0, 0, 0);
+                }
+                __syncthreads();
+            }
+            #pragma unroll
+            for (int c = 0; c < 2; ++c) {
+                int n = n0 + wn + c * 16 + ccol;
+                float bj = p.b_eff[n];
+                #pragma unroll
+                for (int i = 0; i < 4; ++i) {
+                    size_t m = (size_t)(m0 + wm + crow + i);
+                    p.u_buf[m * 512 + n] = fmaxf(acc[c][i] + bj, 0.f);
+                }
+            }
+        } else {
+            const int idx = w - 512;
+            const int f = idx & 63, b = idx >> 6;
+            const size_t row = (size_t)b * SS + f;
+            const unsigned short* Pb = bb + PB_O;
+            const int c0 = lane * 2, c1 = lane * 2 + 1;
+            const float p1f0 = bf2f(Pb[row * 256 + c0]),       p1f1 = bf2f(Pb[row * 256 + c1]);
+            const float p2f0 = bf2f(Pb[row * 256 + 128 + c0]), p2f1 = bf2f(Pb[row * 256 + 128 + c1]);
+            const float w10 = p.d1W2[c0], w11 = p.d1W2[c1];
+            const float w20 = p.d2W2[c0], w21 = p.d2W2[c1];
+            const float b10 = p.d1b1[c0], b11 = p.d1b1[c1];
+            const float b20 = p.d2b1[c0], b21 = p.d2b1[c1];
+            const float bb1 = p.d1b2[0], bb2 = p.d2b2[0];
+            const float* a1r = p.x1_attn + row * SS;
+            const float* ph0 = p.pws + (((size_t)b * 4 + 0) * 64 + f) * 64;
+            const float* ph1 = p.pws + (((size_t)b * 4 + 1) * 64 + f) * 64;
+            const float* ph2 = p.pws + (((size_t)b * 4 + 2) * 64 + f) * 64;
+            const float* ph3 = p.pws + (((size_t)b * 4 + 3) * 64 + f) * 64;
+            const size_t bbase = (size_t)b * SS * 256;
+            for (int g = wave; g < 64; g += 4) {
+                float aa1 = a1r[g];
+                float aa2 = 0.25f * (ph0[g] + ph1[g] + ph2[g] + ph3[g]);
+                float q10 = bf2f(Pb[bbase + g * 256 + c0]);
+                float q11 = bf2f(Pb[bbase + g * 256 + c1]);
+                float q20 = bf2f(Pb[bbase + g * 256 + 128 + c0]);
+                float q21 = bf2f(Pb[bbase + g * 256 + 128 + c1]);
+                float h10 = fmaxf(aa1 * (q10 - p1f0) + b10, 0.f);
+                float h11 = fmaxf(aa1 * (q11 - p1f1) + b11, 0.f);
+                float h20 = fmaxf(aa2 * (q20 - p2f0) + b20, 0.f);
+                float h21 = fmaxf(aa2 * (q21 - p2f1) + b21, 0.f);
+                float s1 = w10 * h10 + w11 * h11;
+                float s2 = w20 * h20 + w21 * h21;
+                #pragma unroll
+                for (int m = 32; m; m >>= 1) {
+                    s1 += __shfl_xor(s1, m);
+                    s2 += __shfl_xor(s2, m);
+                }
+                if (lane == 0) {
+                    p.x2_attn[row * SS + g] = aa2;
+                    p.diff1[row * SS + g] = fmaxf(s1 + bb1, 0.f);
+                    p.diff2[row * SS + g] = fmaxf(s2 + bb2, 0.f);
+                }
+            }
+        }
+        __syncthreads();
+    }
+    grid.sync();
+
+    {
+        float* ssum = (float*)(smem + 27648);
+        float* ssq  = ssum + 4;
+        for (int w = blockIdx.x; w < 2048; w += GS)
+            ln_row(w, p.x, p.u_buf, p.g1, p.be1, p.h_buf, bb + HB_O, ssum, ssq);
+    }
+    grid.sync();
+
+    for (int w = blockIdx.x; w < 512; w += GS) {
+        unsigned short* Asl = (unsigned short*)smem;
+        unsigned short* Bsl = Asl + 2048;
+        const unsigned short* A = bb + HB_O;
+        const unsigned short* B = bb + W2B_O;
+        const int m0 = (w >> 3) * 32, n0 = (w & 7) * 64;
+        const int wm = (wave >> 1) * 16, wn = (wave & 1) * 32;
+        f32x4 acc[2] = {};
+        for (int k0 = 0; k0 < 512; k0 += 64) {
+            {
+                int r = tid >> 3, q = tid & 7;
+                int col = (q ^ (r & 7)) * 8;
+                __builtin_amdgcn_global_load_lds(
+                    (cv_global*)(A + (size_t)(m0 + r) * 512 + k0 + col),
+                    (v_lds*)(Asl + wave * 512), 16, 0, 0);
+            }
+            #pragma unroll
+            for (int c0 = 0; c0 < 512; c0 += 256) {
+                int cc = c0 + tid, r = cc >> 3, q = cc & 7;
+                int col = (q ^ (r & 7)) * 8;
+                __builtin_amdgcn_global_load_lds(
+                    (cv_global*)(B + (size_t)(n0 + r) * 512 + k0 + col),
+                    (v_lds*)(Bsl + c0 * 8 + wave * 512), 16, 0, 0);
+            }
+            __syncthreads();
+            #pragma unroll
+            for (int j = 0; j < 2; ++j) {
+                int kc = (lane >> 4) + j * 4;
+                int rb0 = wn + fr, rb1 = wn + 16 + fr, ra = wm + fr;
+                bf16x8 b0 = *(const bf16x8*)(Bsl + rb0 * 64 + (kc ^ (rb0 & 7)) * 8);
+                bf16x8 b1 = *(const bf16x8*)(Bsl + rb1 * 64 + (kc ^ (rb1 & 7)) * 8);
+                bf16x8 af = *(const bf16x8*)(Asl + ra * 64 + (kc ^ (ra & 7)) * 8);
+                acc[0] = MFMA16(af, b0, acc[0], 0, 0, 0);
+                acc[1] = MFMA16(af, b1, acc[1], 0, 0, 0);
+            }
+            __syncthreads();
+        }
+        #pragma unroll
+        for (int c = 0; c < 2; ++c) {
+            int n = n0 + wn + c * 16 + ccol;
+            float bj = p.b2[n];
+            #pragma unroll
+            for (int i = 0; i < 4; ++i) {
+                size_t m = (size_t)(m0 + wm + crow + i);
+                p.u_buf[m * 512 + n] = fmaxf(acc[c][i] + bj, 0.f);
+            }
+        }
+        __syncthreads();
+    }
+    grid.sync();
+
+    {
+        float* ssum = (float*)(smem + 27648);
+        float* ssq  = ssum + 4;
+        for (int w = blockIdx.x; w < 2048; w += GS)
+            ln_row(w, p.h_buf, p.u_buf, p.g2, p.be2, p.out_main, nullptr, ssum, ssq);
+    }
 }
 
 extern "C" void kernel_launch(void* const* d_in, const int* in_sizes, int n_in,
                               void* d_out, int out_size, void* d_ws,
                               size_t ws_size, hipStream_t stream) {
-    const float* x    = (const float*)d_in[0];
-    const float* Wqkv = (const float*)d_in[1];
-    const float* bqkv = (const float*)d_in[2];
-    const float* Wo   = (const float*)d_in[3];
-    const float* bo   = (const float*)d_in[4];
-    const float* W1   = (const float*)d_in[5];
-    const float* b1   = (const float*)d_in[6];
-    const float* W2   = (const float*)d_in[7];
-    const float* b2   = (const float*)d_in[8];
-    const float* g1   = (const float*)d_in[9];
-    const float* be1  = (const float*)d_in[10];
-    const float* g2   = (const float*)d_in[11];
-    const float* be2  = (const float*)d_in[12];
-    const float* d1W1 = (const float*)d_in[13];
-    const float* d1b1 = (const float*)d_in[14];
-    const float* d1W2 = (const float*)d_in[15];
-    const float* d1b2 = (const float*)d_in[16];
-    const float* d2W1 = (const float*)d_in[17];
-    const float* d2b1 = (const float*)d_in[18];
-    const float* d2W2 = (const float*)d_in[19];
-    const float* d2b2 = (const float*)d_in[20];
-
-    float* out      = (float*)d_out;
-    float* out_main = out;
-    float* x1_attn  = out + 1048576;
-    float* x2_attn  = out + 1048576 + 131072;
-    float* diff1    = out + 1048576 + 2 * 131072;
-    float* diff2    = out + 1048576 + 3 * 131072;
-
-    float* ws    = (float*)d_ws;
-    float* u_buf = ws;
-    float* h_buf = ws + 1048576;
-    float* pws   = ws + 2097152;
-    float* b_eff = ws + 2621440;
-    unsigned short* Pl2 = (unsigned short*)(ws + 2621952);
-    unsigned short* bb  = (unsigned short*)(ws + 2687488);
-
-    unsigned short* xb    = bb + XB_O;
-    unsigned short* Wfull = bb + WFULL_O;
-    unsigned short* W1cb  = bb + W1CB_O;
-    unsigned short* W2b   = bb + W2B_O;
-    unsigned short* qkvb  = bb + QKVB_O;
-    unsigned short* x1o   = bb + X1O_O;
-    unsigned short* hb    = bb + HB_O;
-    unsigned short* Pb    = bb + PB_O;
-
-    mega1<<<1508, 256, 0, stream>>>(x, Wqkv, Wo, W1, W2, d1W1, d2W1, b1, bo,
-                                    bb, b_eff, x1_attn, Pl2);
-
-    gemm_qkvp<<<dim3(36, 32), 256, 0, stream>>>(xb, Wfull, bqkv, qkvb, Pb,
-                                                Pl2, x1o);
-
-    mha_attn<<<dim3(8, 32), 256, 0, stream>>>(qkvb, x1o, pws);
-
-    w1pair<<<2560, 256, 0, stream>>>(x1o, W1cb, b_eff, u_buf, Pb, x1_attn, pws,
-                                     d1b1, d1W2, d1b2, d2b1, d2W2, d2b2,
-                                     x2_attn, diff1, diff2);
-
-    add_ln<<<2048, 256, 0, stream>>>(x, u_buf, g1, be1, h_buf, hb);
-
-    gemm_w2<<<dim3(8, 64), 256, 0, stream>>>(hb, W2b, b2, u_buf);
-
-    add_ln<<<2048, 256, 0, stream>>>(h_buf, u_buf, g2, be2, out_main, nullptr);
+    float* out = (float*)d_out;
+    float* ws  = (float*)d_ws;
+
+    KParams p;
+    p.x    = (const float*)d_in[0];
+    p.Wqkv = (const float*)d_in[1];
+    p.bqkv = (const float*)d_in[2];
+    p.Wo   = (const float*)d_in[3];
+    p.bo   = (const float*)d_in[4];
+    p.W1   = (const float*)d_in[5];
+    p.b1   = (const float*)d_in[6];
+    p.W2   = (const float*)d_in[7];
+    p.b2   = (const float*)d_in[8];
+    p.g1   = (const float*)d_in[9];
+    p.be1  = (const float*)d_in[10];
+    p.g2   = (const float*)d_in[11];
+    p.be2  = (const float*)d_in[12];
+    p.d1W1 = (const float*)d_in[13];
+    p.d1b1 = (const float*)d_in[14];
+    p.d1W2 = (const float*)d_in[15];
+    p.d1b2 = (const float*)d_in[16];
+    p.d2W1 = (const float*)d_in[17];
+    p.d2b1 = (const float*)d_in[18];
+    p.d2W2 = (const float*)d_in[19];
+    p.d2b2 = (const float*)d_in[20];
+
+    p.out_main = out;
+    p.x1_attn  = out + 1048576;
+    p.x2_attn  = out + 1048576 + 131072;
+    p.diff1    = out + 1048576 + 2 * 131072;
+    p.diff2    = out + 1048576 + 3 * 131072;
+
+    p.u_buf = ws;
+    p.h_buf = ws + 1048576;
+    p.pws   = ws + 2097152;
+    p.b_eff = ws + 2621440;
+    p.Pl2   = (unsigned short*)(ws + 2621952);
+    p.bb    = (unsigned short*)(ws + 2687488);
+
+    int maxB = 0;
+    hipOccupancyMaxActiveBlocksPerMultiprocessor(&maxB, (const void*)fused,
+                                                 256, 0);
+    if (maxB < 1) maxB = 1;
+    int grid = maxB * 256;
+    if (grid > 1024) grid = 1024;
+
+    void* kargs[] = { (void*)&p };
+    hipLaunchCooperativeKernel((const void*)fused, dim3(grid), dim3(256),
+                               kargs, 0, stream);
 }
```

New measurement: 577.1 us. +222.5%, slower.
